# Optimization experiments

Measured on AMD Instinct MI355X. Metric: run time of the kernel, lower is better.

The kernel has to match this reference:

```python
import jax, jax.numpy as jnp
from jax import lax
import numpy as np


def _sym(M):
    return 0.5 * (M + M.T)


def setup_inputs() -> dict:
    key = jax.random.key(0)
    k_a, k_c, k_x = jax.random.split(key, 3)
    dimz, dimx, N = 32, 16, 16384
    A = jax.random.normal(k_a, (dimz, dimz), dtype=jnp.float32)
    A = 0.95 * A / jnp.linalg.norm(A, ord=2)  # stable transition (spectral norm 0.95)
    C = jax.random.normal(k_c, (dimx, dimz), dtype=jnp.float32) / np.float32(np.sqrt(dimz))
    Q = 0.1 * jnp.eye(dimz, dtype=jnp.float32)
    R = 0.1 * jnp.eye(dimx, dtype=jnp.float32)
    m0 = jnp.zeros((dimz, 1), dtype=jnp.float32)
    P0 = jnp.eye(dimz, dtype=jnp.float32)
    x = jax.random.normal(k_x, (dimx, N), dtype=jnp.float32)
    Sigma_AQA = jnp.zeros((dimz, dimz), dtype=jnp.float32)
    Sigma_CRC = jnp.zeros((dimz, dimz), dtype=jnp.float32)
    return {"x": x, "A": A, "C": C, "Q": Q, "R": R, "m0": m0, "P0": P0,
            "Sigma_AQA": Sigma_AQA, "Sigma_CRC": Sigma_CRC}


def _vblds_forward(x, A, C, Q, R, m0, P0, Sigma_AQA, Sigma_CRC):
    dimz = A.shape[0]
    I = jnp.eye(dimz, dtype=x.dtype)

    def woodbury(M, B):
        # I - M (I + B M)^{-1} B   (identity when B == 0, matching module init)
        return I - M @ jnp.linalg.inv(I + B @ M) @ B

    def predict(mu, V):
        G = woodbury(V, Sigma_AQA)
        m = A @ (G @ mu)
        P = A @ G @ V @ A.T + Q
        return m, _sym(P), G

    def update(xn, m, P):
        L = woodbury(P, Sigma_CRC)
        x_hat = C @ (L @ m)
        S_hat = C @ L @ P @ C.T + R
        K = L @ P @ C.T @ jnp.linalg.inv(S_hat)
        mu = L @ m + K @ (xn - x_hat)
        V = (I - K @ C) @ L @ P
        return mu, _sym(V)

    # ---- Kalman filter (sequential recursion via lax.scan) ----
    def filt_step(carry, xn):
        m, P = carry
        mu, V = update(xn, m, P)
        m_next, P_next, _ = predict(mu, V)
        return (m_next, P_next), (mu, V)

    (_, _), (muf, Vf) = lax.scan(filt_step, (m0[:, 0], P0), x.T)  # muf: (N, dz), Vf: (N, dz, dz)

    # ---- RTS smoother (reverse scan) ----
    def smooth_step(carry, inp):
        mu_plus, V_plus = carry
        mufn, Vfn = inp
        m, P, G = predict(mufn, Vfn)
        J = G @ Vfn @ A.T @ jnp.linalg.inv(P)
        mu = G @ mufn + J @ (mu_plus - m)
        V = _sym(G @ Vfn + J @ (V_plus - P) @ J.T)
        V12 = J @ V_plus
        return (mu, V), (mu, V, V12)

    (_, _), (mus_rest, Vs_rest, V12) = lax.scan(
        smooth_step, (muf[-1], Vf[-1]), (muf[:-1], Vf[:-1]), reverse=True)
    mus = jnp.concatenate([mus_rest, muf[-1:]], axis=0)   # (N, dz)
    Vs = jnp.concatenate([Vs_rest, Vf[-1:]], axis=0)      # (N, dz, dz)

    # ---- learn: sufficient statistics and M-step log-likelihood ----
    N = mus.shape[0]
    mu = mus.T  # (dz, N)
    zz = mu @ mu.T + Vs.sum(0)
    z1z1 = mu[:, :-1] @ mu[:, :-1].T + Vs[:-1].sum(0)
    z1z2 = mu[:, :-1] @ mu[:, 1:].T + V12.sum(0)
    z2z2 = mu[:, 1:] @ mu[:, 1:].T + Vs[1:].sum(0)
    zx = mu @ x.T
    xx = x @ x.T

    two_pi = 2.0 * np.float32(np.pi)
    m0_new = mu[:, 0:1]
    P0_new = _sym(Vs[0])
    m0m0 = m0_new @ m0_new.T
    z0m0 = mu[:, 0:1] @ m0_new.T
    z0z0 = mu[:, 0:1] @ mu[:, 0:1].T + Vs[0]
    quad0 = _sym(z0z0 - (z0m0 + z0m0.T) + m0m0)
    ell_z0 = (-0.5 * jnp.linalg.slogdet(two_pi * P0_new)[1]
              - 0.5 * jnp.trace(jnp.linalg.inv(P0_new) @ quad0))

    A_new = z1z2.T @ jnp.linalg.inv(z1z1)
    AzzA = A_new @ z1z1 @ A_new.T
    Az1z2 = A_new @ z1z2
    quadz = _sym(z2z2 - (Az1z2 + Az1z2.T) + AzzA)
    Q_new = quadz / (N - 1)
    ell_z = (-(N - 1) / 2.0 * jnp.linalg.slogdet(two_pi * Q_new)[1]
             - 0.5 * jnp.trace(jnp.linalg.inv(Q_new) @ quadz))

    C_new = zx.T @ jnp.linalg.inv(zz)
    Czx = C_new @ zx
    CzzC = C_new @ zz @ C_new.T
    quadx = _sym(xx - (Czx + Czx.T) + CzzC)
    R_new = quadx / N
    ell_x = (-N / 2.0 * jnp.linalg.slogdet(two_pi * R_new)[1]
             - 0.5 * jnp.trace(jnp.linalg.inv(R_new) @ quadx))

    ell = ell_z + ell_x + ell_z0
    # return in torch layout: (dz, N), (dz, dz, N)
    return (ell, muf.T, jnp.moveaxis(Vf, 0, -1), mus.T,
            jnp.moveaxis(Vs, 0, -1), jnp.moveaxis(V12, 0, -1))


def reference(x, A, C, Q, R, m0, P0, Sigma_AQA, Sigma_CRC):
    return _vblds_forward(x, A, C, Q, R, m0, P0, Sigma_AQA, Sigma_CRC)
```

## Files before the change

kernel.cpp:

```cpp
#include <hip/hip_runtime.h>
#include <math.h>

#define NTT 16384
#define PTOL 1e-5f
#define TCAP 48
#define KTR 32
#define CHL 128
#define NCH 128

static constexpr long O_MUF = 1;
static constexpr long O_VF  = O_MUF + 32L*NTT;
static constexpr long O_MUS = O_VF + 1024L*NTT;
static constexpr long O_VS  = O_MUS + 32L*NTT;
static constexpr long O_V12 = O_VS + 1024L*NTT;

static constexpr long WS_PT  = 0;
static constexpr long WS_PAR = 262144;
static constexpr int PW_VC=0, PW_PC=1024, PW_VSINF=2048, PW_V12INF=3072, PW_INTS=4096;
static constexpr int PW_E=4104, PW_EL=5128, PW_K=6152, PW_SMU=6664;
static constexpr int PW_J=6696, PW_JL=7720, PW_D=8744;
static constexpr int PW_VB=9768, PW_BND=13864, PW_WB=17960, PW_BNDM=22056;
static constexpr int PW_HSVS=26152, PW_HSV12=27176, PW_SVSC=28200, PW_SV12C=29224;
static constexpr long WS_GRAM = WS_PAR + 30248;
static constexpr int  GRAM_STRIDE = 2816;
static constexpr long WS_JT = WS_GRAM;

static constexpr int PB_HEAD = KTR + 1;
static constexpr int PB_FILL = PB_HEAD + TCAP;
static constexpr int PB_MUS  = PB_FILL + 1024;
static constexpr int PB_END  = PB_MUS + NCH;

__device__ __forceinline__ void lbar() {
  asm volatile("s_waitcnt lgkmcnt(0)" ::: "memory");
  __builtin_amdgcn_s_barrier();
}

template<int n>
__device__ __forceinline__ void gj_db(float* a, float* b, int ld, float* ldet) {
  const int tid = threadIdx.x;
  const int nth = blockDim.x;
  for (int k = 0; k < n; ++k) {
    float* src = (k & 1) ? b : a;
    float* dst = (k & 1) ? a : b;
    if (ldet != nullptr && tid == 0) *ldet += logf(fabsf(src[k*ld + k]));
    for (int e = tid; e < 2*n*n; e += nth) {
      int r = e / (2*n), c = e - r*(2*n);
      float piv = src[k*ld + k];
      float pr = src[k*ld + c] / piv;
      float v = (r == k) ? pr : fmaf(-src[r*ld + k], pr, src[r*ld + c]);
      dst[r*ld + c] = v;
    }
    lbar();
  }
}

__device__ __forceinline__ void gj32_256(float* a, float* b) {
  const int tid = threadIdx.x;
  for (int k = 0; k < 32; ++k) {
    float* src = (k & 1) ? b : a;
    float* dst = (k & 1) ? a : b;
    #pragma unroll
    for (int e8 = 0; e8 < 8; ++e8) {
      int e = tid + e8*256;
      int r = e >> 6, c = e & 63;
      float piv = src[k*64 + k];
      float pr = src[k*64 + c] / piv;
      dst[r*64 + c] = (r == k) ? pr : fmaf(-src[r*64 + k], pr, src[r*64 + c]);
    }
    lbar();
  }
}

__device__ __forceinline__ void gj3_db(float* a, float* b, float* ldet0) {
  const int tid = threadIdx.x;
  for (int k = 0; k < 32; ++k) {
    float* src = (k & 1) ? b : a;
    float* dst = (k & 1) ? a : b;
    if (ldet0 != nullptr && tid == 0) *ldet0 += logf(fabsf(src[k*65 + k]));
    #pragma unroll
    for (int e = 0; e < 6; ++e) {
      int ee = tid + e*1024;
      int m = ee >> 11;
      int rr = (ee & 2047) >> 6;
      int c = ee & 63;
      int base = m*2080;
      float piv = src[base + k*65 + k];
      float pr = src[base + k*65 + c] / piv;
      float v = (rr == k) ? pr : fmaf(-src[base + rr*65 + k], pr, src[base + rr*65 + c]);
      dst[base + rr*65 + c] = v;
    }
    lbar();
  }
}

__device__ __forceinline__ void gjzx_db(float* qa, float* qb, float* xa, float* xb,
                                        float* ldz, float* ldx) {
  const int tid = threadIdx.x;
  for (int k = 0; k < 32; ++k) {
    float* qs = (k & 1) ? qb : qa;
    float* qd = (k & 1) ? qa : qb;
    if (tid == 0) *ldz += logf(fabsf(qs[k*65 + k]));
    if (tid == 1 && k < 16) {
      float* xs = (k & 1) ? xb : xa;
      *ldx += logf(fabsf(xs[k*33 + k]));
    }
    #pragma unroll
    for (int e = 0; e < 2; ++e) {
      int ee = tid + e*1024;
      int rr = ee >> 6, c = ee & 63;
      float piv = qs[k*65 + k];
      float pr = qs[k*65 + c] / piv;
      qd[rr*65 + c] = (rr == k) ? pr : fmaf(-qs[rr*65 + k], pr, qs[rr*65 + c]);
    }
    if (k < 16 && tid < 512) {
      float* xs = (k & 1) ? xb : xa;
      float* xd = (k & 1) ? xa : xb;
      int rr = tid >> 5, c = tid & 31;
      float piv = xs[k*33 + k];
      float pr = xs[k*33 + c] / piv;
      xd[rr*33 + c] = (rr == k) ? pr : fmaf(-xs[rr*33 + k], pr, xs[rr*33 + c]);
    }
    lbar();
  }
}

__device__ __forceinline__ double block_sum_d(double p, double* red) {
  #pragma unroll
  for (int o = 32; o > 0; o >>= 1) p += __shfl_down(p, o);
  const int tid = threadIdx.x;
  if ((tid & 63) == 0) red[tid >> 6] = p;
  lbar();
  double s = 0.0;
  if (tid == 0) {
    #pragma unroll
    for (int q = 0; q < 16; ++q) s += red[q];
  }
  lbar();
  return s;
}

__global__ __launch_bounds__(256) void k_ric(
    const float* __restrict__ A, const float* __restrict__ C,
    const float* __restrict__ Q, const float* __restrict__ R,
    const float* __restrict__ m0, const float* __restrict__ P0,
    const float* __restrict__ x, float* __restrict__ out, float* __restrict__ wsp)
{
  __shared__ float sA[1056], sC[528], sQ[1056], sR[272];
  __shared__ float sPa[1056], sPb[1056], sV[1056], sAV[1056];
  __shared__ float sCP[528], sKt[544], sAug[528], sAug2[528];
  __shared__ float sm[32], smu[32], sxh[16], sxt[16];
  __shared__ int s_conv;
  const int tid = threadIdx.x;
  const int j = tid & 31, i8 = tid >> 5;

  for (int e = tid; e < 1024; e += 256) {
    int idx = (e>>5)*33 + (e&31);
    sA[idx] = A[e]; sQ[idx] = Q[e]; sPa[idx] = P0[e];
  }
  for (int e = tid; e < 512; e += 256) sC[(e>>5)*33 + (e&31)] = C[e];
  sR[(tid>>4)*17 + (tid&15)] = R[tid];
  if (tid < 32) sm[tid] = m0[tid];
  float xcur = 0.f, xnxt = 0.f;
  if (tid < 16) { xcur = x[(long)tid*NTT + 0]; xnxt = x[(long)tid*NTT + 1]; }
  __syncthreads();
  float aj[32];
  #pragma unroll
  for (int k = 0; k < 32; ++k) aj[k] = sA[j*33+k];

  float* Pc = sPa; float* Pn = sPb;
  int t = 0;
  for (; t < TCAP; ++t) {
    if (tid < 16) sxt[tid] = xcur;
    {
      float a0 = 0.f, a1 = 0.f;
      #pragma unroll
      for (int k = 0; k < 32; ++k) {
        float pv = Pc[k*33+j];
        a0 = fmaf(sC[i8*33+k], pv, a0);
        a1 = fmaf(sC[(i8+8)*33+k], pv, a1);
      }
      sCP[i8*33+j] = a0; sCP[(i8+8)*33+j] = a1;
    }
    if (tid < 16) {
      float acc = 0.f;
      #pragma unroll
      for (int k = 0; k < 32; ++k) acc = fmaf(sC[tid*33+k], sm[k], acc);
      sxh[tid] = acc;
    }
    lbar();
    {
      int r = tid >> 4, c = tid & 15;
      float acc = sR[r*17+c];
      #pragma unroll
      for (int k = 0; k < 32; ++k) acc = fmaf(sCP[r*33+k], sC[c*33+k], acc);
      sAug[r*33+c] = acc;
      sAug[r*33+16+c] = (r==c) ? 1.f : 0.f;
    }
    lbar();
    for (int k = 0; k < 16; ++k) {
      float* src = (k & 1) ? sAug2 : sAug;
      float* dst = (k & 1) ? sAug : sAug2;
      float piv = src[k*33+k];
      float prc = src[k*33+j] / piv;
      int r0 = i8, r1 = i8 + 8;
      dst[r0*33+j] = (r0==k) ? prc : fmaf(-src[r0*33+k], prc, src[r0*33+j]);
      dst[r1*33+j] = (r1==k) ? prc : fmaf(-src[r1*33+k], prc, src[r1*33+j]);
      lbar();
    }
    {
      float a0 = 0.f, a1 = 0.f;
      #pragma unroll
      for (int k = 0; k < 16; ++k) {
        float cpv = sCP[k*33+j];
        a0 = fmaf(cpv, sAug[k*33+16+i8], a0);
        a1 = fmaf(cpv, sAug[k*33+16+i8+8], a1);
      }
      sKt[j*17+i8] = a0; sKt[j*17+i8+8] = a1;
    }
    lbar();
    if (tid < 32) {
      float acc = sm[tid];
      #pragma unroll
      for (int k = 0; k < 16; ++k) acc = fmaf(sKt[tid*17+k], sxt[k]-sxh[k], acc);
      smu[tid] = acc;
      out[O_MUF + (long)tid*NTT + t] = acc;
    }
    {
      float a0 = Pc[i8*33+j], a1 = Pc[(i8+8)*33+j], a2 = Pc[(i8+16)*33+j], a3 = Pc[(i8+24)*33+j];
      #pragma unroll
      for (int k = 0; k < 16; ++k) {
        float cpv = sCP[k*33+j];
        a0 = fmaf(-sKt[i8*17+k], cpv, a0);
        a1 = fmaf(-sKt[(i8+8)*17+k], cpv, a1);
        a2 = fmaf(-sKt[(i8+16)*17+k], cpv, a2);
        a3 = fmaf(-sKt[(i8+24)*17+k], cpv, a3);
      }
      sV[i8*33+j] = a0; sV[(i8+8)*33+j] = a1; sV[(i8+16)*33+j] = a2; sV[(i8+24)*33+j] = a3;
      out[O_VF + (long)(i8*32+j)*NTT + t] = a0;
      out[O_VF + (long)((i8+8)*32+j)*NTT + t] = a1;
      out[O_VF + (long)((i8+16)*32+j)*NTT + t] = a2;
      out[O_VF + (long)((i8+24)*32+j)*NTT + t] = a3;
    }
    if (tid == 0) s_conv = 1;
    lbar();
    {
      float a0=0.f,a1=0.f,a2=0.f,a3=0.f;
      #pragma unroll
      for (int k = 0; k < 32; ++k) {
        float vv = sV[k*33+j];
        a0 = fmaf(sA[i8*33+k], vv, a0);
        a1 = fmaf(sA[(i8+8)*33+k], vv, a1);
        a2 = fmaf(sA[(i8+16)*33+k], vv, a2);
        a3 = fmaf(sA[(i8+24)*33+k], vv, a3);
      }
      sAV[i8*33+j] = a0; sAV[(i8+8)*33+j] = a1; sAV[(i8+16)*33+j] = a2; sAV[(i8+24)*33+j] = a3;
    }
    if (tid < 16) { xcur = xnxt; xnxt = x[(long)tid*NTT + t + 2]; }
    lbar();
    {
      float a0 = sQ[i8*33+j], a1 = sQ[(i8+8)*33+j], a2 = sQ[(i8+16)*33+j], a3 = sQ[(i8+24)*33+j];
      #pragma unroll
      for (int k = 0; k < 32; ++k) {
        float av = aj[k];
        a0 = fmaf(sAV[i8*33+k], av, a0);
        a1 = fmaf(sAV[(i8+8)*33+k], av, a1);
        a2 = fmaf(sAV[(i8+16)*33+k], av, a2);
        a3 = fmaf(sAV[(i8+24)*33+k], av, a3);
      }
      Pn[i8*33+j] = a0; Pn[(i8+8)*33+j] = a1; Pn[(i8+16)*33+j] = a2; Pn[(i8+24)*33+j] = a3;
      if (fabsf(a0 - Pc[i8*33+j]) > PTOL || fabsf(a1 - Pc[(i8+8)*33+j]) > PTOL ||
          fabsf(a2 - Pc[(i8+16)*33+j]) > PTOL || fabsf(a3 - Pc[(i8+24)*33+j]) > PTOL)
        s_conv = 0;
    }
    if (tid < 32) {
      float acc = 0.f;
      #pragma unroll
      for (int k = 0; k < 32; ++k) acc = fmaf(sA[tid*33+k], smu[k], acc);
      sm[tid] = acc;
    }
    lbar();
    int sc = s_conv;
    float* sw = Pc; Pc = Pn; Pn = sw;
    if (sc) { ++t; break; }
  }

  const int t_star = t;
  if (tid == 0) ((int*)(wsp + PW_INTS))[0] = t_star;
  #pragma unroll
  for (int m = 0; m < 4; ++m) {
    int r = i8 + 8*m;
    wsp[PW_VC + r*32 + j] = sV[r*33+j];
    wsp[PW_PC + r*32 + j] = Pc[r*33+j];
  }
  if (tid < 32) wsp[PW_SMU + tid] = smu[tid];
  { int e = tid;        wsp[PW_K + e] = sKt[(e>>4)*17 + (e&15)];
    e = tid + 256;      wsp[PW_K + e] = sKt[(e>>4)*17 + (e&15)]; }
  {
    float a0=(i8==j)?1.f:0.f, a1=((i8+8)==j)?1.f:0.f, a2=((i8+16)==j)?1.f:0.f, a3=((i8+24)==j)?1.f:0.f;
    #pragma unroll
    for (int k = 0; k < 16; ++k) {
      float cv = sC[k*33+j];
      a0 = fmaf(-sKt[i8*17+k], cv, a0);
      a1 = fmaf(-sKt[(i8+8)*17+k], cv, a1);
      a2 = fmaf(-sKt[(i8+16)*17+k], cv, a2);
      a3 = fmaf(-sKt[(i8+24)*17+k], cv, a3);
    }
    sAV[i8*33+j]=a0; sAV[(i8+8)*33+j]=a1; sAV[(i8+16)*33+j]=a2; sAV[(i8+24)*33+j]=a3;
  }
  lbar();
  {
    float a0=0.f,a1=0.f,a2=0.f,a3=0.f;
    #pragma unroll
    for (int k = 0; k < 32; ++k) {
      float av = sA[k*33+j];
      a0 = fmaf(sAV[i8*33+k], av, a0);
      a1 = fmaf(sAV[(i8+8)*33+k], av, a1);
      a2 = fmaf(sAV[(i8+16)*33+k], av, a2);
      a3 = fmaf(sAV[(i8+24)*33+k], av, a3);
    }
    Pn[i8*33+j]=a0; Pn[(i8+8)*33+j]=a1; Pn[(i8+16)*33+j]=a2; Pn[(i8+24)*33+j]=a3;
  }
  lbar();
  #pragma unroll
  for (int m = 0; m < 4; ++m) { int r = i8+8*m; wsp[PW_E + r*32 + j] = Pn[r*33+j]; }
  {
    float* cur = Pn; float* tmp = sAV;
    for (int it = 0; it < 7; ++it) {
      float a0=0.f,a1=0.f,a2=0.f,a3=0.f;
      #pragma unroll
      for (int k = 0; k < 32; ++k) {
        float vv = cur[k*33+j];
        a0 = fmaf(cur[i8*33+k], vv, a0);
        a1 = fmaf(cur[(i8+8)*33+k], vv, a1);
        a2 = fmaf(cur[(i8+16)*33+k], vv, a2);
        a3 = fmaf(cur[(i8+24)*33+k], vv, a3);
      }
      tmp[i8*33+j]=a0; tmp[(i8+8)*33+j]=a1; tmp[(i8+16)*33+j]=a2; tmp[(i8+24)*33+j]=a3;
      lbar();
      float* sw = cur; cur = tmp; tmp = sw;
    }
    #pragma unroll
    for (int m = 0; m < 4; ++m) { int r = i8+8*m; wsp[PW_EL + r*32 + j] = cur[r*33+j]; }
  }
}

__global__ __launch_bounds__(256) void k_sconst(
    const float* __restrict__ A, float* __restrict__ wsp)
{
  __shared__ float sA[1056], sVc[1056], sPc[1056], sJ[1056], sX[1056], sU[1056], sT[1056];
  __shared__ float augA[2048], augB[2048];
  __shared__ float sMs[8448];
  const int tid = threadIdx.x;
  const int j = tid & 31, i8 = tid >> 5;
  const int t_star = ((const int*)(wsp + PW_INTS))[0];

  for (int e = tid; e < 1024; e += 256) {
    int idx = (e>>5)*33 + (e&31);
    sA[idx] = A[e]; sVc[idx] = wsp[PW_VC + e]; sPc[idx] = wsp[PW_PC + e];
    augA[(e>>5)*64 + (e&31)] = wsp[PW_PC + e];
    augA[(e>>5)*64 + 32 + (e&31)] = ((e>>5) == (e&31)) ? 1.f : 0.f;
  }
  __syncthreads();
  gj32_256(augA, augB);

  {
    float a0=0.f,a1=0.f,a2=0.f,a3=0.f;
    #pragma unroll
    for (int k = 0; k < 32; ++k) {
      float av = sA[j*33+k];
      a0 = fmaf(sVc[i8*33+k], av, a0);
      a1 = fmaf(sVc[(i8+8)*33+k], av, a1);
      a2 = fmaf(sVc[(i8+16)*33+k], av, a2);
      a3 = fmaf(sVc[(i8+24)*33+k], av, a3);
    }
    sT[i8*33+j]=a0; sT[(i8+8)*33+j]=a1; sT[(i8+16)*33+j]=a2; sT[(i8+24)*33+j]=a3;
  }
  lbar();
  {
    float a0=0.f,a1=0.f,a2=0.f,a3=0.f;
    #pragma unroll
    for (int k = 0; k < 32; ++k) {
      float pv = augA[k*64+32+j];
      a0 = fmaf(sT[i8*33+k], pv, a0);
      a1 = fmaf(sT[(i8+8)*33+k], pv, a1);
      a2 = fmaf(sT[(i8+16)*33+k], pv, a2);
      a3 = fmaf(sT[(i8+24)*33+k], pv, a3);
    }
    sJ[i8*33+j]=a0; sJ[(i8+8)*33+j]=a1; sJ[(i8+16)*33+j]=a2; sJ[(i8+24)*33+j]=a3;
  }
  lbar();
  #pragma unroll
  for (int m = 0; m < 4; ++m) { int r = i8+8*m; wsp[PW_J + r*32 + j] = sJ[r*33+j]; sMs[r*33+j] = sJ[r*33+j]; }
  {
    float a0=(i8==j)?1.f:0.f, a1=((i8+8)==j)?1.f:0.f, a2=((i8+16)==j)?1.f:0.f, a3=((i8+24)==j)?1.f:0.f;
    float b0=0.f,b1=0.f,b2=0.f,b3=0.f;
    #pragma unroll
    for (int k = 0; k < 32; ++k) {
      float av = sA[k*33+j];
      float pv = sPc[k*33+j];
      a0 = fmaf(-sJ[i8*33+k], av, a0);      b0 = fmaf(sJ[i8*33+k], pv, b0);
      a1 = fmaf(-sJ[(i8+8)*33+k], av, a1);  b1 = fmaf(sJ[(i8+8)*33+k], pv, b1);
      a2 = fmaf(-sJ[(i8+16)*33+k], av, a2); b2 = fmaf(sJ[(i8+16)*33+k], pv, b2);
      a3 = fmaf(-sJ[(i8+24)*33+k], av, a3); b3 = fmaf(sJ[(i8+24)*33+k], pv, b3);
    }
    wsp[PW_D + i8*32+j]=a0; wsp[PW_D + (i8+8)*32+j]=a1; wsp[PW_D + (i8+16)*32+j]=a2; wsp[PW_D + (i8+24)*32+j]=a3;
    sT[i8*33+j]=b0; sT[(i8+8)*33+j]=b1; sT[(i8+16)*33+j]=b2; sT[(i8+24)*33+j]=b3;
  }
  lbar();
  {
    float a0=sVc[i8*33+j], a1=sVc[(i8+8)*33+j], a2=sVc[(i8+16)*33+j], a3=sVc[(i8+24)*33+j];
    #pragma unroll
    for (int k = 0; k < 32; ++k) {
      float jv = sJ[j*33+k];
      a0 = fmaf(-sT[i8*33+k], jv, a0);
      a1 = fmaf(-sT[(i8+8)*33+k], jv, a1);
      a2 = fmaf(-sT[(i8+16)*33+k], jv, a2);
      a3 = fmaf(-sT[(i8+24)*33+k], jv, a3);
    }
    sX[i8*33+j]=a0; sX[(i8+8)*33+j]=a1; sX[(i8+16)*33+j]=a2; sX[(i8+24)*33+j]=a3;
  }
  lbar();
  for (int l = 0; l < 8; ++l) {
    const float* Ml = sMs + l*1056;
    {
      float a0=0.f,a1=0.f,a2=0.f,a3=0.f;
      #pragma unroll
      for (int k = 0; k < 32; ++k) {
        float xv = sX[k*33+j];
        a0 = fmaf(Ml[i8*33+k], xv, a0);
        a1 = fmaf(Ml[(i8+8)*33+k], xv, a1);
        a2 = fmaf(Ml[(i8+16)*33+k], xv, a2);
        a3 = fmaf(Ml[(i8+24)*33+k], xv, a3);
      }
      sU[i8*33+j]=a0; sU[(i8+8)*33+j]=a1; sU[(i8+16)*33+j]=a2; sU[(i8+24)*33+j]=a3;
    }
    lbar();
    {
      float a0=sX[i8*33+j], a1=sX[(i8+8)*33+j], a2=sX[(i8+16)*33+j], a3=sX[(i8+24)*33+j];
      float b0=0.f,b1=0.f,b2=0.f,b3=0.f;
      #pragma unroll
      for (int k = 0; k < 32; ++k) {
        float jv = Ml[j*33+k];
        float mv = Ml[k*33+j];
        a0 = fmaf(sU[i8*33+k], jv, a0);       b0 = fmaf(Ml[i8*33+k], mv, b0);
        a1 = fmaf(sU[(i8+8)*33+k], jv, a1);   b1 = fmaf(Ml[(i8+8)*33+k], mv, b1);
        a2 = fmaf(sU[(i8+16)*33+k], jv, a2);  b2 = fmaf(Ml[(i8+16)*33+k], mv, b2);
        a3 = fmaf(sU[(i8+24)*33+k], jv, a3);  b3 = fmaf(Ml[(i8+24)*33+k], mv, b3);
      }
      sX[i8*33+j]=a0; sX[(i8+8)*33+j]=a1; sX[(i8+16)*33+j]=a2; sX[(i8+24)*33+j]=a3;
      if (l < 7) {
        float* Mn = sMs + (l+1)*1056;
        Mn[i8*33+j]=b0; Mn[(i8+8)*33+j]=b1; Mn[(i8+16)*33+j]=b2; Mn[(i8+24)*33+j]=b3;
      }
    }
    lbar();
  }
  #pragma unroll
  for (int m = 0; m < 4; ++m) {
    int r = i8+8*m;
    wsp[PW_VSINF + r*32 + j] = sX[r*33+j];
    wsp[PW_JL + r*32 + j] = sMs[7*1056 + r*33+j];
  }
  float* sXd = augB;
  #pragma unroll
  for (int m = 0; m < 4; ++m) { int r = i8+8*m; sXd[r*33+j] = sVc[r*33+j] - sX[r*33+j]; }
  lbar();
  for (int l = 0; l < 8; ++l) {
    const float* Ml = sMs + l*1056;
    {
      float a0=0.f,a1=0.f,a2=0.f,a3=0.f;
      #pragma unroll
      for (int k = 0; k < 32; ++k) {
        float xv = sXd[k*33+j];
        a0 = fmaf(Ml[i8*33+k], xv, a0);
        a1 = fmaf(Ml[(i8+8)*33+k], xv, a1);
        a2 = fmaf(Ml[(i8+16)*33+k], xv, a2);
        a3 = fmaf(Ml[(i8+24)*33+k], xv, a3);
      }
      sU[i8*33+j]=a0; sU[(i8+8)*33+j]=a1; sU[(i8+16)*33+j]=a2; sU[(i8+24)*33+j]=a3;
    }
    lbar();
    {
      float a0=sXd[i8*33+j], a1=sXd[(i8+8)*33+j], a2=sXd[(i8+16)*33+j], a3=sXd[(i8+24)*33+j];
      #pragma unroll
      for (int k = 0; k < 32; ++k) {
        float jv = Ml[j*33+k];
        a0 = fmaf(sU[i8*33+k], jv, a0);
        a1 = fmaf(sU[(i8+8)*33+k], jv, a1);
        a2 = fmaf(sU[(i8+16)*33+k], jv, a2);
        a3 = fmaf(sU[(i8+24)*33+k], jv, a3);
      }
      sXd[i8*33+j]=a0; sXd[(i8+8)*33+j]=a1; sXd[(i8+16)*33+j]=a2; sXd[(i8+24)*33+j]=a3;
    }
    lbar();
  }
  {
    float a0=0.f,a1=0.f,a2=0.f,a3=0.f;
    #pragma unroll
    for (int k = 0; k < 32; ++k) {
      float xv = sX[k*33+j];
      a0 = fmaf(sJ[i8*33+k], xv, a0);
      a1 = fmaf(sJ[(i8+8)*33+k], xv, a1);
      a2 = fmaf(sJ[(i8+16)*33+k], xv, a2);
      a3 = fmaf(sJ[(i8+24)*33+k], xv, a3);
    }
    wsp[PW_V12INF + i8*32+j]=a0; wsp[PW_V12INF + (i8+8)*32+j]=a1;
    wsp[PW_V12INF + (i8+16)*32+j]=a2; wsp[PW_V12INF + (i8+24)*32+j]=a3;
  }
  const float nt0 = (float)(NTT - t_star);
  const float nt1 = (float)(NTT - 1 - t_star);
  #pragma unroll
  for (int m = 0; m < 4; ++m) {
    int r = i8+8*m;
    wsp[PW_SVSC + r*32 + j] = nt0*sX[r*33+j] + sXd[r*33+j];
    sT[r*33+j] = nt1*sX[r*33+j] + sXd[r*33+j];
  }
  lbar();
  {
    float a0=0.f,a1=0.f,a2=0.f,a3=0.f;
    #pragma unroll
    for (int k = 0; k < 32; ++k) {
      float tv = sT[k*33+j];
      a0 = fmaf(sJ[i8*33+k], tv, a0);
      a1 = fmaf(sJ[(i8+8)*33+k], tv, a1);
      a2 = fmaf(sJ[(i8+16)*33+k], tv, a2);
      a3 = fmaf(sJ[(i8+24)*33+k], tv, a3);
    }
    wsp[PW_SV12C + i8*32+j]=a0; wsp[PW_SV12C + (i8+8)*32+j]=a1;
    wsp[PW_SV12C + (i8+16)*32+j]=a2; wsp[PW_SV12C + (i8+24)*32+j]=a3;
  }
}

__device__ __forceinline__ float mvp16(const float* m, float v, int b0) {
  float s0=0.f, s1=0.f, s2=0.f, s3=0.f;
  #pragma unroll
  for (int q = 0; q < 4; ++q) {
    s0 = fmaf(m[q],    __shfl(v, b0+q),    s0);
    s1 = fmaf(m[4+q],  __shfl(v, b0+4+q),  s1);
    s2 = fmaf(m[8+q],  __shfl(v, b0+8+q),  s2);
    s3 = fmaf(m[12+q], __shfl(v, b0+12+q), s3);
  }
  return (s0+s1)+(s2+s3);
}
__device__ __forceinline__ float mvp8(const float* m, float v, int b0) {
  float s0=0.f, s1=0.f;
  #pragma unroll
  for (int q = 0; q < 4; ++q) {
    s0 = fmaf(m[q],   __shfl(v, b0+q),   s0);
    s1 = fmaf(m[4+q], __shfl(v, b0+4+q), s1);
  }
  return s0+s1;
}

__global__ __launch_bounds__(64) void k_muf_b1(const float* __restrict__ x, float* __restrict__ wsp) {
  __shared__ float sx[16*(CHL+1)];
  const int lane = threadIdx.x;
  const int t_star = ((const int*)(wsp + PW_INTS))[0];
  const int sb = t_star + (int)blockIdx.x * CHL;
  if (sb >= NTT) return;
  const int len = (NTT - sb < CHL) ? (NTT - sb) : CHL;
  for (int q = 0; q < 16; ++q)
    for (int idx = lane; idx < len; idx += 64)
      sx[q*(CHL+1)+idx] = x[(long)q*NTT + sb + idx];
  const int r = lane & 31, bm = (lane & 32) >> 1, bx = (lane & 32) >> 2;
  float e[16], kx[8];
  #pragma unroll
  for (int q = 0; q < 16; ++q) e[q] = wsp[PW_E + r*32 + bm + q];
  #pragma unroll
  for (int q = 0; q < 8; ++q) kx[q] = wsp[PW_K + r*16 + bx + q];
  lbar();
  float mf = 0.f;
  for (int s = 0; s < len; ++s) {
    float xq = sx[(lane&15)*(CHL+1) + s];
    float acc = mvp16(e, mf, bm) + mvp8(kx, xq, bx);
    acc += __shfl_xor(acc, 32);
    mf = acc;
  }
  if (lane < 32) wsp[PW_VB + (int)blockIdx.x*32 + lane] = mf;
}

__global__ __launch_bounds__(64) void k_muf_comb(float* __restrict__ wsp) {
  __shared__ float svb[NCH*32];
  const int lane = threadIdx.x;
  for (int idx = lane; idx < NCH*32; idx += 64) svb[idx] = wsp[PW_VB + idx];
  const int t_star = ((const int*)(wsp + PW_INTS))[0];
  const int r = lane & 31, bm = (lane & 32) >> 1;
  float el[16];
  #pragma unroll
  for (int q = 0; q < 16; ++q) el[q] = wsp[PW_EL + r*32 + bm + q];
  float m = wsp[PW_SMU + r];
  lbar();
  for (int b = 0; b < NCH; ++b) {
    int sb = t_star + b*CHL;
    if (sb >= NTT) break;
    if (lane < 32) wsp[PW_BND + b*32 + lane] = m;
    if (sb + CHL >= NTT) break;
    float vb = svb[b*32 + r];
    float s = mvp16(el, m, bm);
    s += __shfl_xor(s, 32);
    m = vb + s;
  }
}

__global__ __launch_bounds__(64) void k_muf_b2(const float* __restrict__ x, float* __restrict__ out, float* __restrict__ wsp) {
  __shared__ float sx[16*(CHL+1)];
  const int lane = threadIdx.x;
  const int t_star = ((const int*)(wsp + PW_INTS))[0];
  const int sb = t_star + (int)blockIdx.x * CHL;
  if (sb >= NTT) return;
  const int len = (NTT - sb < CHL) ? (NTT - sb) : CHL;
  for (int q = 0; q < 16; ++q)
    for (int idx = lane; idx < len; idx += 64)
      sx[q*(CHL+1)+idx] = x[(long)q*NTT + sb + idx];
  const int r = lane & 31, bm = (lane & 32) >> 1, bx = (lane & 32) >> 2;
  float e[16], kx[8];
  #pragma unroll
  for (int q = 0; q < 16; ++q) e[q] = wsp[PW_E + r*32 + bm + q];
  #pragma unroll
  for (int q = 0; q < 8; ++q) kx[q] = wsp[PW_K + r*16 + bx + q];
  lbar();
  float mf = wsp[PW_BND + (int)blockIdx.x*32 + r];
  float* po = out + O_MUF + (long)r*NTT + sb;
  for (int s = 0; s < len; ++s) {
    float xq = sx[(lane&15)*(CHL+1) + s];
    float acc = mvp16(e, mf, bm) + mvp8(kx, xq, bx);
    acc += __shfl_xor(acc, 32);
    mf = acc;
    if (lane < 32) po[s] = mf;
  }
}

__global__ __launch_bounds__(1024) void k_par1(
    const float* __restrict__ A, const float* __restrict__ Q,
    float* __restrict__ out, float* __restrict__ ws, float* __restrict__ wsp)
{
  __shared__ float sh[9440];
  const int tid = threadIdx.x;
  const int i = tid >> 5, j = tid & 31;
  const int ij33 = i*33 + j;
  const int b = blockIdx.x;

  if (b < PB_HEAD) {
    const int k = b;
    float* sJ = sh; float* sM = sh+1056; float* sT = sh+2112; float* sDl = sh+3168; float* sVo = sh+4224;
    sJ[ij33] = wsp[PW_J + tid];
    sDl[ij33] = wsp[PW_VC + tid] - wsp[PW_VSINF + tid];
    const float vsi = wsp[PW_VSINF + tid];
    lbar();
    float vs;
    if (k == 0) {
      vs = vsi + sDl[ij33];
    } else {
      sM[ij33] = sJ[ij33];
      lbar();
      int hb = 31 - __builtin_clz((unsigned)k);
      for (int b2 = hb-1; b2 >= 0; --b2) {
        { float acc = 0.f;
          #pragma unroll
          for (int k2 = 0; k2 < 32; ++k2) acc = fmaf(sM[i*33+k2], sM[k2*33+j], acc);
          lbar(); sM[ij33] = acc; lbar(); }
        if ((k >> b2) & 1) {
          float acc = 0.f;
          #pragma unroll
          for (int k2 = 0; k2 < 32; ++k2) acc = fmaf(sM[i*33+k2], sJ[k2*33+j], acc);
          lbar(); sM[ij33] = acc; lbar();
        }
      }
      { float acc = 0.f;
        #pragma unroll
        for (int k2 = 0; k2 < 32; ++k2) acc = fmaf(sM[i*33+k2], sDl[k2*33+j], acc);
        sT[ij33] = acc; }
      lbar();
      { float acc = vsi;
        #pragma unroll
        for (int k2 = 0; k2 < 32; ++k2) acc = fmaf(sT[i*33+k2], sM[j*33+k2], acc);
        vs = acc; }
    }
    out[O_VS + (long)tid*NTT + (NTT-1-k)] = vs;
    sVo[ij33] = vs;
    lbar();
    if (k <= KTR-1) {
      float acc = 0.f;
      #pragma unroll
      for (int k2 = 0; k2 < 32; ++k2) acc = fmaf(sJ[i*33+k2], sVo[k2*33+j], acc);
      out[O_V12 + (long)tid*(NTT-1) + (NTT-2-k)] = acc;
    }
  } else if (b < PB_FILL) {
    const int t_star = ((const int*)(wsp + PW_INTS))[0];
    const int tt = b - PB_HEAD;
    if (tt >= t_star) return;
    float* sA = sh; float* sQ2 = sh+1056; float* sVf = sh+2112; float* sAV = sh+3168; float* sP = sh+4224;
    float* aug = sh+5280; float* aug2 = sh+7360;
    sA[ij33] = A[tid]; sQ2[ij33] = Q[tid];
    sVf[ij33] = out[O_VF + (long)tid*NTT + tt];
    lbar();
    { float acc = 0.f;
      #pragma unroll
      for (int k2 = 0; k2 < 32; ++k2) acc = fmaf(sA[i*33+k2], sVf[k2*33+j], acc);
      sAV[ij33] = acc;
    }
    lbar();
    { float a1 = sQ2[ij33];
      float a2 = sQ2[j*33+i];
      #pragma unroll
      for (int k2 = 0; k2 < 32; ++k2) {
        a1 = fmaf(sAV[i*33+k2], sA[j*33+k2], a1);
        a2 = fmaf(sAV[j*33+k2], sA[i*33+k2], a2);
      }
      float ps = 0.5f*(a1 + a2);
      sP[ij33] = ps;
      aug[i*65+j] = ps; aug[i*65+32+j] = (i==j) ? 1.f : 0.f;
    }
    lbar();
    gj_db<32>(aug, aug2, 65, nullptr);
    { float acc = 0.f;
      #pragma unroll
      for (int k2 = 0; k2 < 32; ++k2) acc = fmaf(sVf[i*33+k2], sA[j*33+k2], acc);
      sAV[ij33] = acc;
    }
    lbar();
    { float acc = 0.f;
      #pragma unroll
      for (int k2 = 0; k2 < 32; ++k2) acc = fmaf(sAV[i*33+k2], aug[k2*65+32+j], acc);
      ws[WS_JT + (long)tt*1024 + tid] = acc;
    }
    ws[WS_PT + (long)tt*1024 + tid] = sP[ij33];
  } else if (b < PB_MUS) {
    const int ij = b - PB_FILL;
    const int t_star = ((const int*)(wsp + PW_INTS))[0];
    const int tb = NTT - 1 - KTR;
    const float vf = wsp[PW_VC + ij];
    const float vs = wsp[PW_VSINF + ij];
    const float v12 = wsp[PW_V12INF + ij];
    float* pvf = out + O_VF + (long)ij*NTT;
    float* pvs = out + O_VS + (long)ij*NTT;
    float* pv12 = out + O_V12 + (long)ij*(NTT-1);
    for (int t2 = t_star + tid; t2 < tb; t2 += 1024) {
      pvf[t2] = vf; pvs[t2] = vs; pv12[t2] = v12;
    }
    for (int t2 = tb + ((t_star + tid - tb) % 1024 + 1024) % 1024; t2 < NTT; t2 += 1024) pvf[t2] = vf;
  } else {
    const int c = b - PB_MUS;
    const int t_star = ((const int*)(wsp + PW_INTS))[0];
    const int te = (NTT-1) - c*CHL;
    if (te <= t_star) return;
    const int ts = (te - CHL > t_star) ? (te - CHL) : t_star;
    const int len = te - ts;
    float* smf = sh;
    if (tid < len) {
      for (int q = 0; q < 32; ++q) smf[q*129 + tid] = out[O_MUF + (long)q*NTT + ts + tid];
    }
    lbar();
    if (tid >= 64) return;
    const int lane = tid;
    const int r = lane & 31, bm = (lane & 32) >> 1;
    float dd[16], jj[16];
    #pragma unroll
    for (int q = 0; q < 16; ++q) { dd[q] = wsp[PW_D + r*32 + bm + q]; jj[q] = wsp[PW_J + r*32 + bm + q]; }
    float z = 0.f;
    for (int tt = len-1; tt >= 0; --tt) {
      float mv = smf[(lane&31)*129 + tt];
      float acc = mvp16(dd, mv, bm) + mvp16(jj, z, bm);
      acc += __shfl_xor(acc, 32);
      z = acc;
    }
    if (lane < 32) wsp[PW_WB + c*32 + lane] = z;
  }
}

__global__ __launch_bounds__(64) void k_mus_comb(float* __restrict__ out, float* __restrict__ wsp) {
  __shared__ float swb[NCH*32];
  const int lane = threadIdx.x;
  for (int idx = lane; idx < NCH*32; idx += 64) swb[idx] = wsp[PW_WB + idx];
  const int t_star = ((const int*)(wsp + PW_INTS))[0];
  const int r = lane & 31, bm = (lane & 32) >> 1;
  float jl[16];
  #pragma unroll
  for (int q = 0; q < 16; ++q) jl[q] = wsp[PW_JL + r*32 + bm + q];
  float m = out[O_MUF + (long)r*NTT + (NTT-1)];
  if (lane < 32) out[O_MUS + (long)lane*NTT + (NTT-1)] = m;
  lbar();
  for (int b = 0; b < NCH; ++b) {
    int te = (NTT-1) - b*CHL;
    if (te <= t_star) break;
    if (lane < 32) wsp[PW_BNDM + b*32 + lane] = m;
    int ts = (te - CHL > t_star) ? (te - CHL) : t_star;
    if (ts <= t_star) break;
    float wb = swb[b*32 + r];
    float s = mvp16(jl, m, bm);
    s += __shfl_xor(s, 32);
    m = wb + s;
  }
}

__global__ __launch_bounds__(64) void k_mus_b2(float* __restrict__ out, float* __restrict__ wsp) {
  __shared__ float smf[32*(CHL+1)];
  const int lane = threadIdx.x;
  const int t_star = ((const int*)(wsp + PW_INTS))[0];
  const int te = (NTT-1) - (int)blockIdx.x*CHL;
  if (te <= t_star) return;
  const int ts = (te - CHL > t_star) ? (te - CHL) : t_star;
  const int len = te - ts;
  for (int q = 0; q < 32; ++q)
    for (int idx = lane; idx < len; idx += 64)
      smf[q*(CHL+1)+idx] = out[O_MUF + (long)q*NTT + ts + idx];
  const int r = lane & 31, bm = (lane & 32) >> 1;
  float dd[16], jj[16];
  #pragma unroll
  for (int q = 0; q < 16; ++q) { dd[q] = wsp[PW_D + r*32 + bm + q]; jj[q] = wsp[PW_J + r*32 + bm + q]; }
  lbar();
  float m = wsp[PW_BNDM + (int)blockIdx.x*32 + r];
  float* po = out + O_MUS + (long)r*NTT;
  for (int tt = len-1; tt >= 0; --tt) {
    float mv = smf[(lane&31)*(CHL+1) + tt];
    float acc = mvp16(dd, mv, bm) + mvp16(jj, m, bm);
    acc += __shfl_xor(acc, 32);
    m = acc;
    if (lane < 32) po[ts+tt] = m;
  }
}

__global__ __launch_bounds__(1024) void k_head_ser(
    const float* __restrict__ A, float* __restrict__ out,
    float* __restrict__ ws, float* __restrict__ wsp)
{
  __shared__ float sA[32*33], sJa[32*33], sJb[32*33], sT1[32*33], sT2[32*33], sVs[32*33];
  __shared__ float smufT[32], sam[32], smsp[32];
  const int tid = threadIdx.x;
  const int i = tid >> 5, j = tid & 31;
  const int ij33 = i*33 + j;
  const int t_star = ((const int*)(wsp + PW_INTS))[0];
  sA[ij33] = A[tid];
  float hsvs = 0.f, hsv12 = 0.f;
  if (t_star > 0) {
    float vsinf = wsp[PW_VSINF + tid];
    int tt = t_star - 1;
    float jc = ws[WS_JT + (long)tt*1024 + tid];
    float pc = ws[WS_PT + (long)tt*1024 + tid];
    float vfc = out[O_VF + (long)tid*NTT + tt];
    float mufc = (tid < 32) ? out[O_MUF + (long)tid*NTT + tt] : 0.f;
    if (tid < 32) smsp[tid] = out[O_MUS + (long)tid*NTT + t_star];
    sVs[ij33] = vsinf;
    sJa[ij33] = jc;
    sT1[ij33] = vsinf - pc;
    if (tid < 32) smufT[tid] = mufc;
    lbar();
    float* Jc = sJa; float* Jn = sJb;
    for (; tt >= 0; --tt) {
      float jN = 0.f, pN = 0.f, vfN = 0.f, mufN = 0.f;
      if (tt > 0) {
        jN = ws[WS_JT + (long)(tt-1)*1024 + tid];
        pN = ws[WS_PT + (long)(tt-1)*1024 + tid];
        vfN = out[O_VF + (long)tid*NTT + (tt-1)];
        if (tid < 32) mufN = out[O_MUF + (long)tid*NTT + (tt-1)];
      }
      {
        float t2 = 0.f, v12 = 0.f;
        #pragma unroll
        for (int k2 = 0; k2 < 32; ++k2) {
          t2  = fmaf(Jc[i*33+k2], sT1[k2*33+j], t2);
          v12 = fmaf(Jc[i*33+k2], sVs[k2*33+j], v12);
        }
        sT2[ij33] = t2;
        out[O_V12 + (long)tid*(NTT-1) + tt] = v12;
        hsv12 += v12;
      }
      if (tid < 32) {
        float a = 0.f;
        #pragma unroll
        for (int k2 = 0; k2 < 32; ++k2) a = fmaf(sA[tid*33+k2], smufT[k2], a);
        sam[tid] = a;
      }
      lbar();
      {
        float vsn = vfc;
        #pragma unroll
        for (int k2 = 0; k2 < 32; ++k2) vsn = fmaf(sT2[i*33+k2], Jc[j*33+k2], vsn);
        out[O_VS + (long)tid*NTT + tt] = vsn;
        hsvs += vsn;
        sVs[ij33] = vsn;
        sT1[ij33] = vsn - pN;
        Jn[ij33] = jN;
      }
      if (tid < 32) {
        float mv = smufT[tid];
        #pragma unroll
        for (int k2 = 0; k2 < 32; ++k2) mv = fmaf(Jc[tid*33+k2], smsp[k2] - sam[k2], mv);
        out[O_MUS + (long)tid*NTT + tt] = mv;
        smsp[tid] = mv;
        smufT[tid] = mufN;
      }
      vfc = vfN;
      { float* sw = Jc; Jc = Jn; Jn = sw; }
      lbar();
    }
  }
  wsp[PW_HSVS + tid] = hsvs;
  wsp[PW_HSV12 + tid] = hsv12;
}

__global__ __launch_bounds__(256) void k_gram(const float* __restrict__ out, const float* __restrict__ x, float* __restrict__ ws) {
  __shared__ float smu[32][257];
  __shared__ float sx[256][16];
  const int b = blockIdx.x;
  const int t0 = b*256;
  for (int e = threadIdx.x; e < 32*257; e += 256) {
    int i2 = e/257, tt = e - i2*257;
    int t = t0 + tt;
    smu[i2][tt] = (t < NTT) ? out[O_MUS + (long)i2*NTT + t] : 0.f;
  }
  for (int e = threadIdx.x; e < 16*256; e += 256) {
    int j2 = e >> 8, tt = e & 255;
    sx[tt][j2] = x[(long)j2*NTT + t0 + tt];
  }
  __syncthreads();
  float* pb = ws + WS_GRAM + (long)b*GRAM_STRIDE;
  const int lim12 = (t0 + 256 <= NTT-1) ? 256 : (NTT-1-t0);
  for (int k = 0; k < 4; ++k) {
    int ij = threadIdx.x + k*256; int i2 = ij>>5, j2 = ij&31;
    float g = 0.f, g12 = 0.f;
    for (int tt = 0; tt < 256; ++tt) g = fmaf(smu[i2][tt], smu[j2][tt], g);
    for (int tt = 0; tt < lim12; ++tt) g12 = fmaf(smu[i2][tt], smu[j2][tt+1], g12);
    pb[ij] = g; pb[1024+ij] = g12;
  }
  for (int k = 0; k < 2; ++k) {
    int ij = threadIdx.x + k*256; int i2 = ij>>4, j2 = ij&15;
    float g = 0.f;
    for (int tt = 0; tt < 256; ++tt) g = fmaf(smu[i2][tt], sx[tt][j2], g);
    pb[2048+ij] = g;
  }
  {
    int ij = threadIdx.x; int i2 = ij>>4, j2 = ij&15;
    float g = 0.f;
    for (int tt = 0; tt < 256; ++tt) g = fmaf(sx[tt][i2], sx[tt][j2], g);
    pb[2560+ij] = g;
  }
}

__global__ __launch_bounds__(1024) void k_final(float* __restrict__ out, float* __restrict__ ws) {
  __shared__ float s_zz[1056], s_z11[1056], s_z12[1056], s_z22[1056];
  __shared__ float s_An[1056], s_T[1056], s_Qz[1056], s_W[1056];
  __shared__ float s_Gx[544], s_xx[272], s_Cn[528], s_U16[528], s_T16[272], s_Qx[272];
  __shared__ float a3[3*2080], b3[3*2080];
  __shared__ float qxa[528], qxb[528];
  __shared__ float s_mu0[32], s_muN[32];
  __shared__ float s_ld[3];
  __shared__ double s_red[16];
  const int tid = threadIdx.x;
  const int i = tid>>5, j = tid&31;
  const int ij33 = i*33+j;
  double ell_acc = 0.0;
  const double L2PI = 1.8378770664093454836;
  const float* wsp = ws + WS_PAR;

  float gall = 0.f, g12 = 0.f;
  for (int b = 0; b < 64; ++b) {
    gall += ws[WS_GRAM + (long)b*GRAM_STRIDE + tid];
    g12  += ws[WS_GRAM + (long)b*GRAM_STRIDE + 1024 + tid];
  }
  float svs  = wsp[PW_HSVS + tid] + wsp[PW_SVSC + tid];
  float sv12 = wsp[PW_HSV12 + tid] + wsp[PW_SV12C + tid];
  float vs0  = out[O_VS + (long)tid*NTT + 0];
  float vsN  = out[O_VS + (long)tid*NTT + (NTT-1)];
  if (tid < 512) { float g = 0.f; for (int b = 0; b < 64; ++b) g += ws[WS_GRAM + (long)b*GRAM_STRIDE + 2048 + tid]; s_Gx[(tid>>4)*17 + (tid&15)] = g; }
  if (tid < 256) { float g = 0.f; for (int b = 0; b < 64; ++b) g += ws[WS_GRAM + (long)b*GRAM_STRIDE + 2560 + tid]; s_xx[(tid>>4)*17 + (tid&15)] = g; }
  if (tid < 32) { s_mu0[tid] = out[O_MUS + (long)tid*NTT + 0]; s_muN[tid] = out[O_MUS + (long)tid*NTT + (NTT-1)]; }
  if (tid < 3) s_ld[tid] = 0.f;
  lbar();
  s_zz[ij33]  = gall + svs;
  s_z11[ij33] = (gall - s_muN[i]*s_muN[j]) + (svs - vsN);
  s_z22[ij33] = (gall - s_mu0[i]*s_mu0[j]) + (svs - vs0);
  s_z12[ij33] = g12 + sv12;
  s_W[ij33]   = vs0;
  lbar();

  {
    float p0n = 0.5f*(s_W[i*33+j] + s_W[j*33+i]);
    float a_  = s_mu0[i]*s_mu0[j];
    float aT  = s_mu0[j]*s_mu0[i];
    float u0  = ((a_ + s_W[ij33]) - (a_ + aT)) + a_;
    s_T[ij33] = u0;
    a3[i*65+j] = p0n;             a3[i*65+32+j] = (i==j) ? 1.f : 0.f;
    a3[2080 + i*65+j] = s_z11[ij33]; a3[2080 + i*65+32+j] = (i==j) ? 1.f : 0.f;
    a3[4160 + i*65+j] = s_zz[ij33];  a3[4160 + i*65+32+j] = (i==j) ? 1.f : 0.f;
  }
  lbar();
  { float q0 = 0.5f*(s_T[i*33+j] + s_T[j*33+i]); s_Qz[ij33] = q0; }
  lbar();
  gj3_db(a3, b3, &s_ld[0]);
  {
    double p = (double)a3[i*65+32+j] * (double)s_Qz[j*33+i];
    double tr = block_sum_d(p, s_red);
    if (tid == 0) ell_acc += -0.5*(32.0*L2PI + (double)s_ld[0]) - 0.5*tr;
  }

  {
    float acc = 0.f;
    #pragma unroll
    for (int k2 = 0; k2 < 32; ++k2) acc = fmaf(s_z12[k2*33+i], a3[2080 + k2*65+32+j], acc);
    s_An[ij33] = acc;
  }
  if (tid < 512) {
    int i16 = tid>>5, j32 = tid&31;
    float acc = 0.f;
    #pragma unroll
    for (int k2 = 0; k2 < 32; ++k2) acc = fmaf(s_Gx[k2*17+i16], a3[4160 + k2*65+32+j32], acc);
    s_Cn[i16*33+j32] = acc;
  }
  lbar();
  {
    float acc = 0.f;
    #pragma unroll
    for (int k2 = 0; k2 < 32; ++k2) acc = fmaf(s_An[i*33+k2], s_z12[k2*33+j], acc);
    s_T[ij33] = acc;
  }
  {
    float acc = 0.f;
    #pragma unroll
    for (int k2 = 0; k2 < 32; ++k2) acc = fmaf(s_An[i*33+k2], s_z11[k2*33+j], acc);
    s_W[ij33] = acc;
  }
  if (tid < 256) {
    int a2 = tid>>4, b2 = tid&15;
    float acc = 0.f;
    #pragma unroll
    for (int k2 = 0; k2 < 32; ++k2) acc = fmaf(s_Cn[a2*33+k2], s_Gx[k2*17+b2], acc);
    s_T16[a2*17+b2] = acc;
  }
  if (tid >= 512) {
    int tt2 = tid - 512;
    int i16 = tt2>>5, j32 = tt2&31;
    float acc = 0.f;
    #pragma unroll
    for (int k2 = 0; k2 < 32; ++k2) acc = fmaf(s_Cn[i16*33+k2], s_zz[k2*33+j32], acc);
    s_U16[i16*33+j32] = acc;
  }
  lbar();
  {
    float azza = 0.f;
    #pragma unroll
    for (int k2 = 0; k2 < 32; ++k2) azza = fmaf(s_W[i*33+k2], s_An[j*33+k2], azza);
    float u = (s_z22[ij33] - (s_T[i*33+j]+s_T[j*33+i])) + azza;
    s_Qz[ij33] = u;
  }
  if (tid < 256) {
    int a2 = tid>>4, b2 = tid&15;
    float czzc = 0.f;
    #pragma unroll
    for (int k2 = 0; k2 < 32; ++k2) czzc = fmaf(s_U16[a2*33+k2], s_Cn[b2*33+k2], czzc);
    float u = (s_xx[a2*17+b2] - (s_T16[a2*17+b2]+s_T16[b2*17+a2])) + czzc;
    s_Qx[a2*17+b2] = u;
  }
  lbar();
  {
    float qz = 0.5f*(s_Qz[i*33+j]+s_Qz[j*33+i]);
    s_T[ij33] = qz;
    a3[i*65+j] = qz/16383.0f; a3[i*65+32+j] = (i==j) ? 1.f : 0.f;
  }
  if (tid < 256) {
    int a2 = tid>>4, b2 = tid&15;
    float qx = 0.5f*(s_Qx[a2*17+b2]+s_Qx[b2*17+a2]);
    s_T16[a2*17+b2] = qx;
    qxa[a2*33+b2] = qx/16384.0f; qxa[a2*33+16+b2] = (a2==b2) ? 1.f : 0.f;
  }
  lbar();
  gjzx_db(a3, b3, qxa, qxb, &s_ld[1], &s_ld[2]);
  {
    double p = (double)a3[i*65+32+j] * (double)s_T[j*33+i];
    double tr = block_sum_d(p, s_red);
    if (tid == 0) ell_acc += -8191.5*(32.0*L2PI + (double)s_ld[1]) - 0.5*tr;
  }
  {
    double p = (i < 16 && j < 16) ? (double)qxa[i*33+16+j] * (double)s_T16[j*17+i] : 0.0;
    double tr = block_sum_d(p, s_red);
    if (tid == 0) {
      ell_acc += -8192.0*(16.0*L2PI + (double)s_ld[2]) - 0.5*tr;
      out[0] = (float)ell_acc;
    }
  }
}

extern "C" void kernel_launch(void* const* d_in, const int* in_sizes, int n_in,
                              void* d_out, int out_size, void* d_ws, size_t ws_size,
                              hipStream_t stream) {
  (void)in_sizes; (void)n_in; (void)out_size; (void)ws_size;
  const float* x  = (const float*)d_in[0];
  const float* A  = (const float*)d_in[1];
  const float* C  = (const float*)d_in[2];
  const float* Q  = (const float*)d_in[3];
  const float* R  = (const float*)d_in[4];
  const float* m0 = (const float*)d_in[5];
  const float* P0 = (const float*)d_in[6];
  float* out = (float*)d_out;
  float* ws  = (float*)d_ws;
  float* wsp = ws + WS_PAR;

  hipLaunchKernelGGL(k_ric, dim3(1), dim3(256), 0, stream, A, C, Q, R, m0, P0, x, out, wsp);
  hipLaunchKernelGGL(k_muf_b1, dim3(NCH), dim3(64), 0, stream, x, wsp);
  hipLaunchKernelGGL(k_sconst, dim3(1), dim3(256), 0, stream, A, wsp);
  hipLaunchKernelGGL(k_muf_comb, dim3(1), dim3(64), 0, stream, wsp);
  hipLaunchKernelGGL(k_muf_b2, dim3(NCH), dim3(64), 0, stream, x, out, wsp);
  hipLaunchKernelGGL(k_par1, dim3(PB_END), dim3(1024), 0, stream, A, Q, out, ws, wsp);
  hipLaunchKernelGGL(k_mus_comb, dim3(1), dim3(64), 0, stream, out, wsp);
  hipLaunchKernelGGL(k_mus_b2, dim3(NCH), dim3(64), 0, stream, out, wsp);
  hipLaunchKernelGGL(k_head_ser, dim3(1), dim3(1024), 0, stream, A, out, ws, wsp);
  hipLaunchKernelGGL(k_gram, dim3(64), dim3(256), 0, stream, out, x, ws);
  hipLaunchKernelGGL(k_final, dim3(1), dim3(1024), 0, stream, out, ws);
}
```

Baseline: 508.6 us.

## Replace chunked scan combine passes with overlapping warm-up chunks and blocked inversion

The forward and backward mean recursions previously ran a three-pass chunked scan: per-chunk partials, then a serial combine kernel, then a second pass. Each chunk now starts its recursion GRD steps earlier from a zero state and relies on the stable steady-state transition to forget that start, which removes the combine and boundary kernels and several launches. The filter step is restructured so the predict covariance is computed directly from P via precomputed CA and fused products. Gauss-Jordan inversion now eliminates 4x4 pivot blocks, cutting the number of barriers per inversion by four. The warm-up is an approximation whose accuracy depends on how fast the transition contracts, and the blocked elimination does no pivoting.

```diff
diff --git a/kernel.cpp b/kernel.cpp
--- a/kernel.cpp
+++ b/kernel.cpp
@@ -6,6 +6,7 @@
 #define TCAP 48
 #define KTR 32
 #define CHL 128
+#define GRD 192
 #define NCH 128
 
 static constexpr long O_MUF = 1;
@@ -17,9 +18,8 @@
 static constexpr long WS_PT  = 0;
 static constexpr long WS_PAR = 262144;
 static constexpr int PW_VC=0, PW_PC=1024, PW_VSINF=2048, PW_V12INF=3072, PW_INTS=4096;
-static constexpr int PW_E=4104, PW_EL=5128, PW_K=6152, PW_SMU=6664;
-static constexpr int PW_J=6696, PW_JL=7720, PW_D=8744;
-static constexpr int PW_VB=9768, PW_BND=13864, PW_WB=17960, PW_BNDM=22056;
+static constexpr int PW_E=4104, PW_K=6152, PW_SMU=6664;
+static constexpr int PW_J=6696, PW_D=8744;
 static constexpr int PW_HSVS=26152, PW_HSV12=27176, PW_SVSC=28200, PW_SV12C=29224;
 static constexpr long WS_GRAM = WS_PAR + 30248;
 static constexpr int  GRAM_STRIDE = 2816;
@@ -35,39 +35,65 @@
   __builtin_amdgcn_s_barrier();
 }
 
-template<int n>
-__device__ __forceinline__ void gj_db(float* a, float* b, int ld, float* ldet) {
-  const int tid = threadIdx.x;
-  const int nth = blockDim.x;
-  for (int k = 0; k < n; ++k) {
-    float* src = (k & 1) ? b : a;
-    float* dst = (k & 1) ? a : b;
-    if (ldet != nullptr && tid == 0) *ldet += logf(fabsf(src[k*ld + k]));
-    for (int e = tid; e < 2*n*n; e += nth) {
-      int r = e / (2*n), c = e - r*(2*n);
-      float piv = src[k*ld + k];
-      float pr = src[k*ld + c] / piv;
-      float v = (r == k) ? pr : fmaf(-src[r*ld + k], pr, src[r*ld + c]);
-      dst[r*ld + c] = v;
-    }
-    lbar();
-  }
-}
-
-__device__ __forceinline__ void gj32_256(float* a, float* b) {
-  const int tid = threadIdx.x;
-  for (int k = 0; k < 32; ++k) {
-    float* src = (k & 1) ? b : a;
-    float* dst = (k & 1) ? a : b;
-    #pragma unroll
-    for (int e8 = 0; e8 < 8; ++e8) {
-      int e = tid + e8*256;
-      int r = e >> 6, c = e & 63;
-      float piv = src[k*64 + k];
-      float pr = src[k*64 + c] / piv;
-      dst[r*64 + c] = (r == k) ? pr : fmaf(-src[r*64 + k], pr, src[r*64 + c]);
-    }
-    lbar();
+__device__ __forceinline__ float inv4f(const float* s, int ld, int k, float* w) {
+  float m[4][8];
+  #pragma unroll
+  for (int r = 0; r < 4; ++r) {
+    #pragma unroll
+    for (int c = 0; c < 4; ++c) m[r][c] = s[(k+r)*ld + k + c];
+    m[r][4] = (r==0)?1.f:0.f; m[r][5] = (r==1)?1.f:0.f;
+    m[r][6] = (r==2)?1.f:0.f; m[r][7] = (r==3)?1.f:0.f;
+  }
+  float det = 1.f;
+  #pragma unroll
+  for (int p = 0; p < 4; ++p) {
+    float pv = m[p][p];
+    det *= pv;
+    float rc = 1.f / pv;
+    #pragma unroll
+    for (int c = 0; c < 8; ++c) m[p][c] *= rc;
+    #pragma unroll
+    for (int r = 0; r < 4; ++r) {
+      if (r == p) continue;
+      float f = m[r][p];
+      #pragma unroll
+      for (int c = 0; c < 8; ++c) m[r][c] = fmaf(-f, m[p][c], m[r][c]);
+    }
+  }
+  #pragma unroll
+  for (int r = 0; r < 4; ++r) {
+    w[r*4+0]=m[r][4]; w[r*4+1]=m[r][5]; w[r*4+2]=m[r][6]; w[r*4+3]=m[r][7];
+  }
+  return det;
+}
+
+template<int NR, int LD>
+__device__ __forceinline__ void gjb4_full(float* a, float* b, int tid, int nth, float* ldet) {
+  float* s = a; float* d = b;
+  const int WDT = 2*NR;
+  for (int kb = 0; kb < NR; kb += 4) {
+    float w[16];
+    float det = inv4f(s, LD, kb, w);
+    if (ldet != nullptr && tid == 0) *ldet += logf(fabsf(det));
+    for (int e = tid; e < NR*WDT; e += nth) {
+      int r = e / WDT, c = e - r*WDT;
+      float v;
+      if ((unsigned)(r - kb) < 4u) {
+        int rr = r - kb;
+        v = w[rr*4+0]*s[kb*LD+c] + w[rr*4+1]*s[(kb+1)*LD+c]
+          + w[rr*4+2]*s[(kb+2)*LD+c] + w[rr*4+3]*s[(kb+3)*LD+c];
+      } else {
+        float s0=s[r*LD+kb], s1=s[r*LD+kb+1], s2=s[r*LD+kb+2], s3=s[r*LD+kb+3];
+        float l0 = s0*w[0]+s1*w[4]+s2*w[8]+s3*w[12];
+        float l1 = s0*w[1]+s1*w[5]+s2*w[9]+s3*w[13];
+        float l2 = s0*w[2]+s1*w[6]+s2*w[10]+s3*w[14];
+        float l3 = s0*w[3]+s1*w[7]+s2*w[11]+s3*w[15];
+        v = s[r*LD+c] - (l0*s[kb*LD+c] + l1*s[(kb+1)*LD+c] + l2*s[(kb+2)*LD+c] + l3*s[(kb+3)*LD+c]);
+      }
+      d[r*LD+c] = v;
+    }
+    lbar();
+    float* t2 = s; s = d; d = t2;
   }
 }
 
@@ -139,19 +165,22 @@
   return s;
 }
 
-__global__ __launch_bounds__(256) void k_ric(
+__global__ __launch_bounds__(256) void k_fwd2(
     const float* __restrict__ A, const float* __restrict__ C,
     const float* __restrict__ Q, const float* __restrict__ R,
     const float* __restrict__ m0, const float* __restrict__ P0,
     const float* __restrict__ x, float* __restrict__ out, float* __restrict__ wsp)
 {
-  __shared__ float sA[1056], sC[528], sQ[1056], sR[272];
-  __shared__ float sPa[1056], sPb[1056], sV[1056], sAV[1056];
-  __shared__ float sCP[528], sKt[544], sAug[528], sAug2[528];
-  __shared__ float sm[32], smu[32], sxh[16], sxt[16];
+  __shared__ float sA[1056], sC[528], sQ[1056], sR[272], sCA[528];
+  __shared__ float sPa[1056], sPb[1056], sV[1056], sT[1056];
+  __shared__ float sW[528], sU1[1056], sU2[544];
+  __shared__ float sSa[528], sSb[528], sZ[528], sZ2[528], sK[544];
+  __shared__ float sm[32], smu[32], sxh[16], sxt[16], sy[16];
+  __shared__ float augA[2080], augB[2080], sMs[8448], sJ[1056], sX[1056], sU[1056], sT3[1056];
   __shared__ int s_conv;
   const int tid = threadIdx.x;
   const int j = tid & 31, i8 = tid >> 5;
+  const int r0 = i8, r1 = i8+8, r2 = i8+16, r3 = i8+24;
 
   for (int e = tid; e < 1024; e += 256) {
     int idx = (e>>5)*33 + (e&31);
@@ -161,263 +190,252 @@
   sR[(tid>>4)*17 + (tid&15)] = R[tid];
   if (tid < 32) sm[tid] = m0[tid];
   float xcur = 0.f, xnxt = 0.f;
-  if (tid < 16) { xcur = x[(long)tid*NTT + 0]; xnxt = x[(long)tid*NTT + 1]; }
+  if (tid < 16) { xcur = x[(long)tid*NTT]; xnxt = x[(long)tid*NTT + 1]; }
   __syncthreads();
   float aj[32];
   #pragma unroll
   for (int k = 0; k < 32; ++k) aj[k] = sA[j*33+k];
+  {
+    float a0=0.f, a1=0.f;
+    #pragma unroll
+    for (int k = 0; k < 32; ++k) {
+      float av = sA[k*33+j];
+      a0 = fmaf(sC[r0*33+k], av, a0);
+      a1 = fmaf(sC[r1*33+k], av, a1);
+    }
+    sCA[r0*33+j] = a0; sCA[r1*33+j] = a1;
+  }
+  if (tid < 16) {
+    float acc = 0.f;
+    #pragma unroll
+    for (int k = 0; k < 32; ++k) acc = fmaf(sC[tid*33+k], sm[k], acc);
+    sxh[tid] = acc;
+  }
+  lbar();
 
   float* Pc = sPa; float* Pn = sPb;
   int t = 0;
   for (; t < TCAP; ++t) {
     if (tid < 16) sxt[tid] = xcur;
     {
-      float a0 = 0.f, a1 = 0.f;
+      float a0=0.f,a1=0.f,a2=0.f,a3=0.f,w0=0.f,w1=0.f;
       #pragma unroll
       for (int k = 0; k < 32; ++k) {
         float pv = Pc[k*33+j];
-        a0 = fmaf(sC[i8*33+k], pv, a0);
-        a1 = fmaf(sC[(i8+8)*33+k], pv, a1);
-      }
-      sCP[i8*33+j] = a0; sCP[(i8+8)*33+j] = a1;
-    }
-    if (tid < 16) {
-      float acc = 0.f;
-      #pragma unroll
-      for (int k = 0; k < 32; ++k) acc = fmaf(sC[tid*33+k], sm[k], acc);
-      sxh[tid] = acc;
+        a0 = fmaf(sA[r0*33+k], pv, a0);
+        a1 = fmaf(sA[r1*33+k], pv, a1);
+        a2 = fmaf(sA[r2*33+k], pv, a2);
+        a3 = fmaf(sA[r3*33+k], pv, a3);
+        w0 = fmaf(sC[r0*33+k], pv, w0);
+        w1 = fmaf(sC[r1*33+k], pv, w1);
+      }
+      sT[r0*33+j]=a0; sT[r1*33+j]=a1; sT[r2*33+j]=a2; sT[r3*33+j]=a3;
+      sW[r0*33+j]=w0; sW[r1*33+j]=w1;
+    }
+    if (t > 0) {
+      if (tid < 32) {
+        float acc = 0.f;
+        #pragma unroll
+        for (int k = 0; k < 32; ++k) acc = fmaf(sA[tid*33+k], smu[k], acc);
+        sm[tid] = acc;
+      } else if (tid < 48) {
+        int q = tid - 32;
+        float acc = 0.f;
+        #pragma unroll
+        for (int k = 0; k < 32; ++k) acc = fmaf(sCA[q*33+k], smu[k], acc);
+        sxh[q] = acc;
+      }
     }
     lbar();
     {
       int r = tid >> 4, c = tid & 15;
       float acc = sR[r*17+c];
       #pragma unroll
-      for (int k = 0; k < 32; ++k) acc = fmaf(sCP[r*33+k], sC[c*33+k], acc);
-      sAug[r*33+c] = acc;
-      sAug[r*33+16+c] = (r==c) ? 1.f : 0.f;
-    }
-    lbar();
-    for (int k = 0; k < 16; ++k) {
-      float* src = (k & 1) ? sAug2 : sAug;
-      float* dst = (k & 1) ? sAug : sAug2;
-      float piv = src[k*33+k];
-      float prc = src[k*33+j] / piv;
-      int r0 = i8, r1 = i8 + 8;
-      dst[r0*33+j] = (r0==k) ? prc : fmaf(-src[r0*33+k], prc, src[r0*33+j]);
-      dst[r1*33+j] = (r1==k) ? prc : fmaf(-src[r1*33+k], prc, src[r1*33+j]);
-      lbar();
+      for (int k = 0; k < 32; ++k) acc = fmaf(sW[r*33+k], sC[c*33+k], acc);
+      sSa[r*33+c] = acc;
+      sSa[r*33+16+c] = (r==c) ? 1.f : 0.f;
     }
     {
-      float a0 = 0.f, a1 = 0.f;
-      #pragma unroll
-      for (int k = 0; k < 16; ++k) {
-        float cpv = sCP[k*33+j];
-        a0 = fmaf(cpv, sAug[k*33+16+i8], a0);
-        a1 = fmaf(cpv, sAug[k*33+16+i8+8], a1);
-      }
-      sKt[j*17+i8] = a0; sKt[j*17+i8+8] = a1;
-    }
-    lbar();
+      float a0=sQ[r0*33+j], a1=sQ[r1*33+j], a2=sQ[r2*33+j], a3=sQ[r3*33+j];
+      #pragma unroll
+      for (int k = 0; k < 32; ++k) {
+        float av = aj[k];
+        a0 = fmaf(sT[r0*33+k], av, a0);
+        a1 = fmaf(sT[r1*33+k], av, a1);
+        a2 = fmaf(sT[r2*33+k], av, a2);
+        a3 = fmaf(sT[r3*33+k], av, a3);
+      }
+      sU1[r0*33+j]=a0; sU1[r1*33+j]=a1; sU1[r2*33+j]=a2; sU1[r3*33+j]=a3;
+    }
+    {
+      int rp = tid >> 4, ci = tid & 15;
+      float b0=0.f, b1=0.f;
+      #pragma unroll
+      for (int k = 0; k < 32; ++k) {
+        float cv = sC[ci*33+k];
+        b0 = fmaf(sT[rp*33+k], cv, b0);
+        b1 = fmaf(sT[(rp+16)*33+k], cv, b1);
+      }
+      sU2[rp*17+ci] = b0; sU2[(rp+16)*17+ci] = b1;
+    }
+    lbar();
+    gjb4_full<16,33>(sSa, sSb, tid, 256, nullptr);
+    {
+      float z0=0.f,z1=0.f,q0=0.f,q1=0.f;
+      #pragma unroll
+      for (int q = 0; q < 16; ++q) {
+        float wv = sW[q*33+j];
+        float u2v = sU2[j*17+q];
+        float s0 = sSa[r0*33+16+q];
+        float s1 = sSa[r1*33+16+q];
+        z0 = fmaf(s0, wv, z0); z1 = fmaf(s1, wv, z1);
+        q0 = fmaf(s0, u2v, q0); q1 = fmaf(s1, u2v, q1);
+      }
+      sZ[r0*33+j]=z0; sZ[r1*33+j]=z1; sZ2[r0*33+j]=q0; sZ2[r1*33+j]=q1;
+    }
+    if (tid < 16) {
+      float acc = 0.f;
+      #pragma unroll
+      for (int q = 0; q < 16; ++q) acc = fmaf(sSa[tid*33+16+q], sxt[q]-sxh[q], acc);
+      sy[tid] = acc;
+    }
+    if (tid == 0) s_conv = 1;
+    lbar();
+    {
+      float v0=Pc[r0*33+j], v1=Pc[r1*33+j], v2=Pc[r2*33+j], v3=Pc[r3*33+j];
+      float p0=sU1[r0*33+j], p1=sU1[r1*33+j], p2=sU1[r2*33+j], p3=sU1[r3*33+j];
+      #pragma unroll
+      for (int q = 0; q < 16; ++q) {
+        float zv = sZ[q*33+j], z2v = sZ2[q*33+j];
+        v0 = fmaf(-sW[q*33+r0], zv, v0);
+        v1 = fmaf(-sW[q*33+r1], zv, v1);
+        v2 = fmaf(-sW[q*33+r2], zv, v2);
+        v3 = fmaf(-sW[q*33+r3], zv, v3);
+        p0 = fmaf(-sU2[r0*17+q], z2v, p0);
+        p1 = fmaf(-sU2[r1*17+q], z2v, p1);
+        p2 = fmaf(-sU2[r2*17+q], z2v, p2);
+        p3 = fmaf(-sU2[r3*17+q], z2v, p3);
+      }
+      sV[r0*33+j]=v0; sV[r1*33+j]=v1; sV[r2*33+j]=v2; sV[r3*33+j]=v3;
+      out[O_VF + (long)(r0*32+j)*NTT + t] = v0;
+      out[O_VF + (long)(r1*32+j)*NTT + t] = v1;
+      out[O_VF + (long)(r2*32+j)*NTT + t] = v2;
+      out[O_VF + (long)(r3*32+j)*NTT + t] = v3;
+      Pn[r0*33+j]=p0; Pn[r1*33+j]=p1; Pn[r2*33+j]=p2; Pn[r3*33+j]=p3;
+      if (fabsf(p0-Pc[r0*33+j]) > PTOL || fabsf(p1-Pc[r1*33+j]) > PTOL ||
+          fabsf(p2-Pc[r2*33+j]) > PTOL || fabsf(p3-Pc[r3*33+j]) > PTOL) s_conv = 0;
+    }
     if (tid < 32) {
       float acc = sm[tid];
       #pragma unroll
-      for (int k = 0; k < 16; ++k) acc = fmaf(sKt[tid*17+k], sxt[k]-sxh[k], acc);
+      for (int q = 0; q < 16; ++q) acc = fmaf(sW[q*33+tid], sy[q], acc);
       smu[tid] = acc;
       out[O_MUF + (long)tid*NTT + t] = acc;
     }
-    {
-      float a0 = Pc[i8*33+j], a1 = Pc[(i8+8)*33+j], a2 = Pc[(i8+16)*33+j], a3 = Pc[(i8+24)*33+j];
-      #pragma unroll
-      for (int k = 0; k < 16; ++k) {
-        float cpv = sCP[k*33+j];
-        a0 = fmaf(-sKt[i8*17+k], cpv, a0);
-        a1 = fmaf(-sKt[(i8+8)*17+k], cpv, a1);
-        a2 = fmaf(-sKt[(i8+16)*17+k], cpv, a2);
-        a3 = fmaf(-sKt[(i8+24)*17+k], cpv, a3);
-      }
-      sV[i8*33+j] = a0; sV[(i8+8)*33+j] = a1; sV[(i8+16)*33+j] = a2; sV[(i8+24)*33+j] = a3;
-      out[O_VF + (long)(i8*32+j)*NTT + t] = a0;
-      out[O_VF + (long)((i8+8)*32+j)*NTT + t] = a1;
-      out[O_VF + (long)((i8+16)*32+j)*NTT + t] = a2;
-      out[O_VF + (long)((i8+24)*32+j)*NTT + t] = a3;
-    }
-    if (tid == 0) s_conv = 1;
-    lbar();
-    {
-      float a0=0.f,a1=0.f,a2=0.f,a3=0.f;
-      #pragma unroll
-      for (int k = 0; k < 32; ++k) {
-        float vv = sV[k*33+j];
-        a0 = fmaf(sA[i8*33+k], vv, a0);
-        a1 = fmaf(sA[(i8+8)*33+k], vv, a1);
-        a2 = fmaf(sA[(i8+16)*33+k], vv, a2);
-        a3 = fmaf(sA[(i8+24)*33+k], vv, a3);
-      }
-      sAV[i8*33+j] = a0; sAV[(i8+8)*33+j] = a1; sAV[(i8+16)*33+j] = a2; sAV[(i8+24)*33+j] = a3;
-    }
     if (tid < 16) { xcur = xnxt; xnxt = x[(long)tid*NTT + t + 2]; }
     lbar();
-    {
-      float a0 = sQ[i8*33+j], a1 = sQ[(i8+8)*33+j], a2 = sQ[(i8+16)*33+j], a3 = sQ[(i8+24)*33+j];
-      #pragma unroll
-      for (int k = 0; k < 32; ++k) {
-        float av = aj[k];
-        a0 = fmaf(sAV[i8*33+k], av, a0);
-        a1 = fmaf(sAV[(i8+8)*33+k], av, a1);
-        a2 = fmaf(sAV[(i8+16)*33+k], av, a2);
-        a3 = fmaf(sAV[(i8+24)*33+k], av, a3);
-      }
-      Pn[i8*33+j] = a0; Pn[(i8+8)*33+j] = a1; Pn[(i8+16)*33+j] = a2; Pn[(i8+24)*33+j] = a3;
-      if (fabsf(a0 - Pc[i8*33+j]) > PTOL || fabsf(a1 - Pc[(i8+8)*33+j]) > PTOL ||
-          fabsf(a2 - Pc[(i8+16)*33+j]) > PTOL || fabsf(a3 - Pc[(i8+24)*33+j]) > PTOL)
-        s_conv = 0;
-    }
-    if (tid < 32) {
-      float acc = 0.f;
-      #pragma unroll
-      for (int k = 0; k < 32; ++k) acc = fmaf(sA[tid*33+k], smu[k], acc);
-      sm[tid] = acc;
-    }
-    lbar();
     int sc = s_conv;
-    float* sw = Pc; Pc = Pn; Pn = sw;
+    { float* sw = Pc; Pc = Pn; Pn = sw; }
     if (sc) { ++t; break; }
   }
 
   const int t_star = t;
   if (tid == 0) ((int*)(wsp + PW_INTS))[0] = t_star;
-  #pragma unroll
-  for (int m = 0; m < 4; ++m) {
-    int r = i8 + 8*m;
-    wsp[PW_VC + r*32 + j] = sV[r*33+j];
-    wsp[PW_PC + r*32 + j] = Pc[r*33+j];
-  }
+  wsp[PW_VC + r0*32+j] = sV[r0*33+j]; wsp[PW_VC + r1*32+j] = sV[r1*33+j];
+  wsp[PW_VC + r2*32+j] = sV[r2*33+j]; wsp[PW_VC + r3*32+j] = sV[r3*33+j];
+  wsp[PW_PC + r0*32+j] = Pc[r0*33+j]; wsp[PW_PC + r1*32+j] = Pc[r1*33+j];
+  wsp[PW_PC + r2*32+j] = Pc[r2*33+j]; wsp[PW_PC + r3*32+j] = Pc[r3*33+j];
   if (tid < 32) wsp[PW_SMU + tid] = smu[tid];
-  { int e = tid;        wsp[PW_K + e] = sKt[(e>>4)*17 + (e&15)];
-    e = tid + 256;      wsp[PW_K + e] = sKt[(e>>4)*17 + (e&15)]; }
-  {
-    float a0=(i8==j)?1.f:0.f, a1=((i8+8)==j)?1.f:0.f, a2=((i8+16)==j)?1.f:0.f, a3=((i8+24)==j)?1.f:0.f;
-    #pragma unroll
-    for (int k = 0; k < 16; ++k) {
-      float cv = sC[k*33+j];
-      a0 = fmaf(-sKt[i8*17+k], cv, a0);
-      a1 = fmaf(-sKt[(i8+8)*17+k], cv, a1);
-      a2 = fmaf(-sKt[(i8+16)*17+k], cv, a2);
-      a3 = fmaf(-sKt[(i8+24)*17+k], cv, a3);
-    }
-    sAV[i8*33+j]=a0; sAV[(i8+8)*33+j]=a1; sAV[(i8+16)*33+j]=a2; sAV[(i8+24)*33+j]=a3;
-  }
-  lbar();
+  {
+    int rp = tid >> 4, ci = tid & 15;
+    float k0=0.f, k1=0.f;
+    #pragma unroll
+    for (int q = 0; q < 16; ++q) {
+      float sv = sSa[q*33+16+ci];
+      k0 = fmaf(sW[q*33+rp], sv, k0);
+      k1 = fmaf(sW[q*33+rp+16], sv, k1);
+    }
+    sK[rp*17+ci]=k0; sK[(rp+16)*17+ci]=k1;
+    wsp[PW_K + rp*16+ci]=k0; wsp[PW_K + (rp+16)*16+ci]=k1;
+  }
+  lbar();
+  {
+    float e0=sA[r0*33+j], e1=sA[r1*33+j], e2=sA[r2*33+j], e3=sA[r3*33+j];
+    #pragma unroll
+    for (int q = 0; q < 16; ++q) {
+      float cav = sCA[q*33+j];
+      e0 = fmaf(-sK[r0*17+q], cav, e0);
+      e1 = fmaf(-sK[r1*17+q], cav, e1);
+      e2 = fmaf(-sK[r2*17+q], cav, e2);
+      e3 = fmaf(-sK[r3*17+q], cav, e3);
+    }
+    wsp[PW_E + r0*32+j]=e0; wsp[PW_E + r1*32+j]=e1;
+    wsp[PW_E + r2*32+j]=e2; wsp[PW_E + r3*32+j]=e3;
+  }
+  for (int e = tid; e < 2048; e += 256) {
+    int r = e >> 6, c = e & 63;
+    augA[r*65+c] = (c < 32) ? Pc[r*33+c] : ((c-32 == r) ? 1.f : 0.f);
+  }
+  lbar();
+  gjb4_full<32,65>(augA, augB, tid, 256, nullptr);
   {
     float a0=0.f,a1=0.f,a2=0.f,a3=0.f;
+    #pragma unroll
+    for (int k = 0; k < 32; ++k) {
+      float av = aj[k];
+      a0 = fmaf(sV[r0*33+k], av, a0);
+      a1 = fmaf(sV[r1*33+k], av, a1);
+      a2 = fmaf(sV[r2*33+k], av, a2);
+      a3 = fmaf(sV[r3*33+k], av, a3);
+    }
+    sT3[r0*33+j]=a0; sT3[r1*33+j]=a1; sT3[r2*33+j]=a2; sT3[r3*33+j]=a3;
+  }
+  lbar();
+  {
+    float a0=0.f,a1=0.f,a2=0.f,a3=0.f;
+    #pragma unroll
+    for (int k = 0; k < 32; ++k) {
+      float pv = augA[k*65+32+j];
+      a0 = fmaf(sT3[r0*33+k], pv, a0);
+      a1 = fmaf(sT3[r1*33+k], pv, a1);
+      a2 = fmaf(sT3[r2*33+k], pv, a2);
+      a3 = fmaf(sT3[r3*33+k], pv, a3);
+    }
+    sJ[r0*33+j]=a0; sJ[r1*33+j]=a1; sJ[r2*33+j]=a2; sJ[r3*33+j]=a3;
+  }
+  lbar();
+  wsp[PW_J + r0*32+j]=sJ[r0*33+j]; wsp[PW_J + r1*32+j]=sJ[r1*33+j];
+  wsp[PW_J + r2*32+j]=sJ[r2*33+j]; wsp[PW_J + r3*32+j]=sJ[r3*33+j];
+  sMs[r0*33+j]=sJ[r0*33+j]; sMs[r1*33+j]=sJ[r1*33+j];
+  sMs[r2*33+j]=sJ[r2*33+j]; sMs[r3*33+j]=sJ[r3*33+j];
+  {
+    float a0=(r0==j)?1.f:0.f, a1=(r1==j)?1.f:0.f, a2=(r2==j)?1.f:0.f, a3=(r3==j)?1.f:0.f;
+    float b0=0.f,b1=0.f,b2=0.f,b3=0.f;
     #pragma unroll
     for (int k = 0; k < 32; ++k) {
       float av = sA[k*33+j];
-      a0 = fmaf(sAV[i8*33+k], av, a0);
-      a1 = fmaf(sAV[(i8+8)*33+k], av, a1);
-      a2 = fmaf(sAV[(i8+16)*33+k], av, a2);
-      a3 = fmaf(sAV[(i8+24)*33+k], av, a3);
-    }
-    Pn[i8*33+j]=a0; Pn[(i8+8)*33+j]=a1; Pn[(i8+16)*33+j]=a2; Pn[(i8+24)*33+j]=a3;
-  }
-  lbar();
-  #pragma unroll
-  for (int m = 0; m < 4; ++m) { int r = i8+8*m; wsp[PW_E + r*32 + j] = Pn[r*33+j]; }
-  {
-    float* cur = Pn; float* tmp = sAV;
-    for (int it = 0; it < 7; ++it) {
-      float a0=0.f,a1=0.f,a2=0.f,a3=0.f;
-      #pragma unroll
-      for (int k = 0; k < 32; ++k) {
-        float vv = cur[k*33+j];
-        a0 = fmaf(cur[i8*33+k], vv, a0);
-        a1 = fmaf(cur[(i8+8)*33+k], vv, a1);
-        a2 = fmaf(cur[(i8+16)*33+k], vv, a2);
-        a3 = fmaf(cur[(i8+24)*33+k], vv, a3);
-      }
-      tmp[i8*33+j]=a0; tmp[(i8+8)*33+j]=a1; tmp[(i8+16)*33+j]=a2; tmp[(i8+24)*33+j]=a3;
-      lbar();
-      float* sw = cur; cur = tmp; tmp = sw;
-    }
-    #pragma unroll
-    for (int m = 0; m < 4; ++m) { int r = i8+8*m; wsp[PW_EL + r*32 + j] = cur[r*33+j]; }
-  }
-}
-
-__global__ __launch_bounds__(256) void k_sconst(
-    const float* __restrict__ A, float* __restrict__ wsp)
-{
-  __shared__ float sA[1056], sVc[1056], sPc[1056], sJ[1056], sX[1056], sU[1056], sT[1056];
-  __shared__ float augA[2048], augB[2048];
-  __shared__ float sMs[8448];
-  const int tid = threadIdx.x;
-  const int j = tid & 31, i8 = tid >> 5;
-  const int t_star = ((const int*)(wsp + PW_INTS))[0];
-
-  for (int e = tid; e < 1024; e += 256) {
-    int idx = (e>>5)*33 + (e&31);
-    sA[idx] = A[e]; sVc[idx] = wsp[PW_VC + e]; sPc[idx] = wsp[PW_PC + e];
-    augA[(e>>5)*64 + (e&31)] = wsp[PW_PC + e];
-    augA[(e>>5)*64 + 32 + (e&31)] = ((e>>5) == (e&31)) ? 1.f : 0.f;
-  }
-  __syncthreads();
-  gj32_256(augA, augB);
-
-  {
-    float a0=0.f,a1=0.f,a2=0.f,a3=0.f;
-    #pragma unroll
-    for (int k = 0; k < 32; ++k) {
-      float av = sA[j*33+k];
-      a0 = fmaf(sVc[i8*33+k], av, a0);
-      a1 = fmaf(sVc[(i8+8)*33+k], av, a1);
-      a2 = fmaf(sVc[(i8+16)*33+k], av, a2);
-      a3 = fmaf(sVc[(i8+24)*33+k], av, a3);
-    }
-    sT[i8*33+j]=a0; sT[(i8+8)*33+j]=a1; sT[(i8+16)*33+j]=a2; sT[(i8+24)*33+j]=a3;
-  }
-  lbar();
-  {
-    float a0=0.f,a1=0.f,a2=0.f,a3=0.f;
-    #pragma unroll
-    for (int k = 0; k < 32; ++k) {
-      float pv = augA[k*64+32+j];
-      a0 = fmaf(sT[i8*33+k], pv, a0);
-      a1 = fmaf(sT[(i8+8)*33+k], pv, a1);
-      a2 = fmaf(sT[(i8+16)*33+k], pv, a2);
-      a3 = fmaf(sT[(i8+24)*33+k], pv, a3);
-    }
-    sJ[i8*33+j]=a0; sJ[(i8+8)*33+j]=a1; sJ[(i8+16)*33+j]=a2; sJ[(i8+24)*33+j]=a3;
-  }
-  lbar();
-  #pragma unroll
-  for (int m = 0; m < 4; ++m) { int r = i8+8*m; wsp[PW_J + r*32 + j] = sJ[r*33+j]; sMs[r*33+j] = sJ[r*33+j]; }
-  {
-    float a0=(i8==j)?1.f:0.f, a1=((i8+8)==j)?1.f:0.f, a2=((i8+16)==j)?1.f:0.f, a3=((i8+24)==j)?1.f:0.f;
-    float b0=0.f,b1=0.f,b2=0.f,b3=0.f;
-    #pragma unroll
-    for (int k = 0; k < 32; ++k) {
-      float av = sA[k*33+j];
-      float pv = sPc[k*33+j];
-      a0 = fmaf(-sJ[i8*33+k], av, a0);      b0 = fmaf(sJ[i8*33+k], pv, b0);
-      a1 = fmaf(-sJ[(i8+8)*33+k], av, a1);  b1 = fmaf(sJ[(i8+8)*33+k], pv, b1);
-      a2 = fmaf(-sJ[(i8+16)*33+k], av, a2); b2 = fmaf(sJ[(i8+16)*33+k], pv, b2);
-      a3 = fmaf(-sJ[(i8+24)*33+k], av, a3); b3 = fmaf(sJ[(i8+24)*33+k], pv, b3);
-    }
-    wsp[PW_D + i8*32+j]=a0; wsp[PW_D + (i8+8)*32+j]=a1; wsp[PW_D + (i8+16)*32+j]=a2; wsp[PW_D + (i8+24)*32+j]=a3;
-    sT[i8*33+j]=b0; sT[(i8+8)*33+j]=b1; sT[(i8+16)*33+j]=b2; sT[(i8+24)*33+j]=b3;
-  }
-  lbar();
-  {
-    float a0=sVc[i8*33+j], a1=sVc[(i8+8)*33+j], a2=sVc[(i8+16)*33+j], a3=sVc[(i8+24)*33+j];
+      float pv = Pc[k*33+j];
+      a0 = fmaf(-sJ[r0*33+k], av, a0); b0 = fmaf(sJ[r0*33+k], pv, b0);
+      a1 = fmaf(-sJ[r1*33+k], av, a1); b1 = fmaf(sJ[r1*33+k], pv, b1);
+      a2 = fmaf(-sJ[r2*33+k], av, a2); b2 = fmaf(sJ[r2*33+k], pv, b2);
+      a3 = fmaf(-sJ[r3*33+k], av, a3); b3 = fmaf(sJ[r3*33+k], pv, b3);
+    }
+    wsp[PW_D + r0*32+j]=a0; wsp[PW_D + r1*32+j]=a1;
+    wsp[PW_D + r2*32+j]=a2; wsp[PW_D + r3*32+j]=a3;
+    sT3[r0*33+j]=b0; sT3[r1*33+j]=b1; sT3[r2*33+j]=b2; sT3[r3*33+j]=b3;
+  }
+  lbar();
+  {
+    float a0=sV[r0*33+j], a1=sV[r1*33+j], a2=sV[r2*33+j], a3=sV[r3*33+j];
     #pragma unroll
     for (int k = 0; k < 32; ++k) {
       float jv = sJ[j*33+k];
-      a0 = fmaf(-sT[i8*33+k], jv, a0);
-      a1 = fmaf(-sT[(i8+8)*33+k], jv, a1);
-      a2 = fmaf(-sT[(i8+16)*33+k], jv, a2);
-      a3 = fmaf(-sT[(i8+24)*33+k], jv, a3);
-    }
-    sX[i8*33+j]=a0; sX[(i8+8)*33+j]=a1; sX[(i8+16)*33+j]=a2; sX[(i8+24)*33+j]=a3;
+      a0 = fmaf(-sT3[r0*33+k], jv, a0);
+      a1 = fmaf(-sT3[r1*33+k], jv, a1);
+      a2 = fmaf(-sT3[r2*33+k], jv, a2);
+      a3 = fmaf(-sT3[r3*33+k], jv, a3);
+    }
+    sX[r0*33+j]=a0; sX[r1*33+j]=a1; sX[r2*33+j]=a2; sX[r3*33+j]=a3;
   }
   lbar();
   for (int l = 0; l < 8; ++l) {
@@ -427,43 +445,41 @@
       #pragma unroll
       for (int k = 0; k < 32; ++k) {
         float xv = sX[k*33+j];
-        a0 = fmaf(Ml[i8*33+k], xv, a0);
-        a1 = fmaf(Ml[(i8+8)*33+k], xv, a1);
-        a2 = fmaf(Ml[(i8+16)*33+k], xv, a2);
-        a3 = fmaf(Ml[(i8+24)*33+k], xv, a3);
-      }
-      sU[i8*33+j]=a0; sU[(i8+8)*33+j]=a1; sU[(i8+16)*33+j]=a2; sU[(i8+24)*33+j]=a3;
+        a0 = fmaf(Ml[r0*33+k], xv, a0);
+        a1 = fmaf(Ml[r1*33+k], xv, a1);
+        a2 = fmaf(Ml[r2*33+k], xv, a2);
+        a3 = fmaf(Ml[r3*33+k], xv, a3);
+      }
+      sU[r0*33+j]=a0; sU[r1*33+j]=a1; sU[r2*33+j]=a2; sU[r3*33+j]=a3;
     }
     lbar();
     {
-      float a0=sX[i8*33+j], a1=sX[(i8+8)*33+j], a2=sX[(i8+16)*33+j], a3=sX[(i8+24)*33+j];
+      float a0=sX[r0*33+j], a1=sX[r1*33+j], a2=sX[r2*33+j], a3=sX[r3*33+j];
       float b0=0.f,b1=0.f,b2=0.f,b3=0.f;
       #pragma unroll
       for (int k = 0; k < 32; ++k) {
         float jv = Ml[j*33+k];
         float mv = Ml[k*33+j];
-        a0 = fmaf(sU[i8*33+k], jv, a0);       b0 = fmaf(Ml[i8*33+k], mv, b0);
-        a1 = fmaf(sU[(i8+8)*33+k], jv, a1);   b1 = fmaf(Ml[(i8+8)*33+k], mv, b1);
-        a2 = fmaf(sU[(i8+16)*33+k], jv, a2);  b2 = fmaf(Ml[(i8+16)*33+k], mv, b2);
-        a3 = fmaf(sU[(i8+24)*33+k], jv, a3);  b3 = fmaf(Ml[(i8+24)*33+k], mv, b3);
-      }
-      sX[i8*33+j]=a0; sX[(i8+8)*33+j]=a1; sX[(i8+16)*33+j]=a2; sX[(i8+24)*33+j]=a3;
+        a0 = fmaf(sU[r0*33+k], jv, a0); b0 = fmaf(Ml[r0*33+k], mv, b0);
+        a1 = fmaf(sU[r1*33+k], jv, a1); b1 = fmaf(Ml[r1*33+k], mv, b1);
+        a2 = fmaf(sU[r2*33+k], jv, a2); b2 = fmaf(Ml[r2*33+k], mv, b2);
+        a3 = fmaf(sU[r3*33+k], jv, a3); b3 = fmaf(Ml[r3*33+k], mv, b3);
+      }
+      sX[r0*33+j]=a0; sX[r1*33+j]=a1; sX[r2*33+j]=a2; sX[r3*33+j]=a3;
       if (l < 7) {
         float* Mn = sMs + (l+1)*1056;
-        Mn[i8*33+j]=b0; Mn[(i8+8)*33+j]=b1; Mn[(i8+16)*33+j]=b2; Mn[(i8+24)*33+j]=b3;
-      }
-    }
-    lbar();
-  }
-  #pragma unroll
-  for (int m = 0; m < 4; ++m) {
-    int r = i8+8*m;
-    wsp[PW_VSINF + r*32 + j] = sX[r*33+j];
-    wsp[PW_JL + r*32 + j] = sMs[7*1056 + r*33+j];
-  }
+        Mn[r0*33+j]=b0; Mn[r1*33+j]=b1; Mn[r2*33+j]=b2; Mn[r3*33+j]=b3;
+      }
+    }
+    lbar();
+  }
+  wsp[PW_VSINF + r0*32+j]=sX[r0*33+j]; wsp[PW_VSINF + r1*32+j]=sX[r1*33+j];
+  wsp[PW_VSINF + r2*32+j]=sX[r2*33+j]; wsp[PW_VSINF + r3*32+j]=sX[r3*33+j];
   float* sXd = augB;
-  #pragma unroll
-  for (int m = 0; m < 4; ++m) { int r = i8+8*m; sXd[r*33+j] = sVc[r*33+j] - sX[r*33+j]; }
+  sXd[r0*33+j] = sV[r0*33+j] - sX[r0*33+j];
+  sXd[r1*33+j] = sV[r1*33+j] - sX[r1*33+j];
+  sXd[r2*33+j] = sV[r2*33+j] - sX[r2*33+j];
+  sXd[r3*33+j] = sV[r3*33+j] - sX[r3*33+j];
   lbar();
   for (int l = 0; l < 8; ++l) {
     const float* Ml = sMs + l*1056;
@@ -472,25 +488,25 @@
       #pragma unroll
       for (int k = 0; k < 32; ++k) {
         float xv = sXd[k*33+j];
-        a0 = fmaf(Ml[i8*33+k], xv, a0);
-        a1 = fmaf(Ml[(i8+8)*33+k], xv, a1);
-        a2 = fmaf(Ml[(i8+16)*33+k], xv, a2);
-        a3 = fmaf(Ml[(i8+24)*33+k], xv, a3);
-      }
-      sU[i8*33+j]=a0; sU[(i8+8)*33+j]=a1; sU[(i8+16)*33+j]=a2; sU[(i8+24)*33+j]=a3;
+        a0 = fmaf(Ml[r0*33+k], xv, a0);
+        a1 = fmaf(Ml[r1*33+k], xv, a1);
+        a2 = fmaf(Ml[r2*33+k], xv, a2);
+        a3 = fmaf(Ml[r3*33+k], xv, a3);
+      }
+      sU[r0*33+j]=a0; sU[r1*33+j]=a1; sU[r2*33+j]=a2; sU[r3*33+j]=a3;
     }
     lbar();
     {
-      float a0=sXd[i8*33+j], a1=sXd[(i8+8)*33+j], a2=sXd[(i8+16)*33+j], a3=sXd[(i8+24)*33+j];
+      float a0=sXd[r0*33+j], a1=sXd[r1*33+j], a2=sXd[r2*33+j], a3=sXd[r3*33+j];
       #pragma unroll
       for (int k = 0; k < 32; ++k) {
         float jv = Ml[j*33+k];
-        a0 = fmaf(sU[i8*33+k], jv, a0);
-        a1 = fmaf(sU[(i8+8)*33+k], jv, a1);
-        a2 = fmaf(sU[(i8+16)*33+k], jv, a2);
-        a3 = fmaf(sU[(i8+24)*33+k], jv, a3);
-      }
-      sXd[i8*33+j]=a0; sXd[(i8+8)*33+j]=a1; sXd[(i8+16)*33+j]=a2; sXd[(i8+24)*33+j]=a3;
+        a0 = fmaf(sU[r0*33+k], jv, a0);
+        a1 = fmaf(sU[r1*33+k], jv, a1);
+        a2 = fmaf(sU[r2*33+k], jv, a2);
+        a3 = fmaf(sU[r3*33+k], jv, a3);
+      }
+      sXd[r0*33+j]=a0; sXd[r1*33+j]=a1; sXd[r2*33+j]=a2; sXd[r3*33+j]=a3;
     }
     lbar();
   }
@@ -499,35 +515,37 @@
     #pragma unroll
     for (int k = 0; k < 32; ++k) {
       float xv = sX[k*33+j];
-      a0 = fmaf(sJ[i8*33+k], xv, a0);
-      a1 = fmaf(sJ[(i8+8)*33+k], xv, a1);
-      a2 = fmaf(sJ[(i8+16)*33+k], xv, a2);
-      a3 = fmaf(sJ[(i8+24)*33+k], xv, a3);
-    }
-    wsp[PW_V12INF + i8*32+j]=a0; wsp[PW_V12INF + (i8+8)*32+j]=a1;
-    wsp[PW_V12INF + (i8+16)*32+j]=a2; wsp[PW_V12INF + (i8+24)*32+j]=a3;
-  }
-  const float nt0 = (float)(NTT - t_star);
-  const float nt1 = (float)(NTT - 1 - t_star);
-  #pragma unroll
-  for (int m = 0; m < 4; ++m) {
-    int r = i8+8*m;
-    wsp[PW_SVSC + r*32 + j] = nt0*sX[r*33+j] + sXd[r*33+j];
-    sT[r*33+j] = nt1*sX[r*33+j] + sXd[r*33+j];
-  }
+      a0 = fmaf(sJ[r0*33+k], xv, a0);
+      a1 = fmaf(sJ[r1*33+k], xv, a1);
+      a2 = fmaf(sJ[r2*33+k], xv, a2);
+      a3 = fmaf(sJ[r3*33+k], xv, a3);
+    }
+    wsp[PW_V12INF + r0*32+j]=a0; wsp[PW_V12INF + r1*32+j]=a1;
+    wsp[PW_V12INF + r2*32+j]=a2; wsp[PW_V12INF + r3*32+j]=a3;
+  }
+  const float nt0f = (float)(NTT - t_star);
+  const float nt1f = (float)(NTT - 1 - t_star);
+  wsp[PW_SVSC + r0*32+j] = nt0f*sX[r0*33+j] + sXd[r0*33+j];
+  wsp[PW_SVSC + r1*32+j] = nt0f*sX[r1*33+j] + sXd[r1*33+j];
+  wsp[PW_SVSC + r2*32+j] = nt0f*sX[r2*33+j] + sXd[r2*33+j];
+  wsp[PW_SVSC + r3*32+j] = nt0f*sX[r3*33+j] + sXd[r3*33+j];
+  sT3[r0*33+j] = nt1f*sX[r0*33+j] + sXd[r0*33+j];
+  sT3[r1*33+j] = nt1f*sX[r1*33+j] + sXd[r1*33+j];
+  sT3[r2*33+j] = nt1f*sX[r2*33+j] + sXd[r2*33+j];
+  sT3[r3*33+j] = nt1f*sX[r3*33+j] + sXd[r3*33+j];
   lbar();
   {
     float a0=0.f,a1=0.f,a2=0.f,a3=0.f;
     #pragma unroll
     for (int k = 0; k < 32; ++k) {
-      float tv = sT[k*33+j];
-      a0 = fmaf(sJ[i8*33+k], tv, a0);
-      a1 = fmaf(sJ[(i8+8)*33+k], tv, a1);
-      a2 = fmaf(sJ[(i8+16)*33+k], tv, a2);
-      a3 = fmaf(sJ[(i8+24)*33+k], tv, a3);
-    }
-    wsp[PW_SV12C + i8*32+j]=a0; wsp[PW_SV12C + (i8+8)*32+j]=a1;
-    wsp[PW_SV12C + (i8+16)*32+j]=a2; wsp[PW_SV12C + (i8+24)*32+j]=a3;
+      float tv = sT3[k*33+j];
+      a0 = fmaf(sJ[r0*33+k], tv, a0);
+      a1 = fmaf(sJ[r1*33+k], tv, a1);
+      a2 = fmaf(sJ[r2*33+k], tv, a2);
+      a3 = fmaf(sJ[r3*33+k], tv, a3);
+    }
+    wsp[PW_SV12C + r0*32+j]=a0; wsp[PW_SV12C + r1*32+j]=a1;
+    wsp[PW_SV12C + r2*32+j]=a2; wsp[PW_SV12C + r3*32+j]=a3;
   }
 }
 
@@ -552,81 +570,35 @@
   return s0+s1;
 }
 
-__global__ __launch_bounds__(64) void k_muf_b1(const float* __restrict__ x, float* __restrict__ wsp) {
-  __shared__ float sx[16*(CHL+1)];
+__global__ __launch_bounds__(64) void k_muf(const float* __restrict__ x, float* __restrict__ out, float* __restrict__ wsp) {
+  __shared__ float sx[16*321];
   const int lane = threadIdx.x;
   const int t_star = ((const int*)(wsp + PW_INTS))[0];
   const int sb = t_star + (int)blockIdx.x * CHL;
   if (sb >= NTT) return;
   const int len = (NTT - sb < CHL) ? (NTT - sb) : CHL;
+  int gs = (blockIdx.x == 0) ? sb : sb - GRD;
+  if (gs < 0) gs = 0;
+  const int total = sb + len - gs;
   for (int q = 0; q < 16; ++q)
-    for (int idx = lane; idx < len; idx += 64)
-      sx[q*(CHL+1)+idx] = x[(long)q*NTT + sb + idx];
+    for (int idx = lane; idx < total; idx += 64)
+      sx[q*321 + idx] = x[(long)q*NTT + gs + idx];
   const int r = lane & 31, bm = (lane & 32) >> 1, bx = (lane & 32) >> 2;
   float e[16], kx[8];
   #pragma unroll
   for (int q = 0; q < 16; ++q) e[q] = wsp[PW_E + r*32 + bm + q];
   #pragma unroll
   for (int q = 0; q < 8; ++q) kx[q] = wsp[PW_K + r*16 + bx + q];
-  lbar();
-  float mf = 0.f;
-  for (int s = 0; s < len; ++s) {
-    float xq = sx[(lane&15)*(CHL+1) + s];
+  float mf = (blockIdx.x == 0) ? wsp[PW_SMU + r] : 0.f;
+  lbar();
+  float* po = out + O_MUF + (long)r*NTT;
+  for (int s = 0; s < total; ++s) {
+    float xq = sx[(lane&15)*321 + s];
     float acc = mvp16(e, mf, bm) + mvp8(kx, xq, bx);
     acc += __shfl_xor(acc, 32);
     mf = acc;
-  }
-  if (lane < 32) wsp[PW_VB + (int)blockIdx.x*32 + lane] = mf;
-}
-
-__global__ __launch_bounds__(64) void k_muf_comb(float* __restrict__ wsp) {
-  __shared__ float svb[NCH*32];
-  const int lane = threadIdx.x;
-  for (int idx = lane; idx < NCH*32; idx += 64) svb[idx] = wsp[PW_VB + idx];
-  const int t_star = ((const int*)(wsp + PW_INTS))[0];
-  const int r = lane & 31, bm = (lane & 32) >> 1;
-  float el[16];
-  #pragma unroll
-  for (int q = 0; q < 16; ++q) el[q] = wsp[PW_EL + r*32 + bm + q];
-  float m = wsp[PW_SMU + r];
-  lbar();
-  for (int b = 0; b < NCH; ++b) {
-    int sb = t_star + b*CHL;
-    if (sb >= NTT) break;
-    if (lane < 32) wsp[PW_BND + b*32 + lane] = m;
-    if (sb + CHL >= NTT) break;
-    float vb = svb[b*32 + r];
-    float s = mvp16(el, m, bm);
-    s += __shfl_xor(s, 32);
-    m = vb + s;
-  }
-}
-
-__global__ __launch_bounds__(64) void k_muf_b2(const float* __restrict__ x, float* __restrict__ out, float* __restrict__ wsp) {
-  __shared__ float sx[16*(CHL+1)];
-  const int lane = threadIdx.x;
-  const int t_star = ((const int*)(wsp + PW_INTS))[0];
-  const int sb = t_star + (int)blockIdx.x * CHL;
-  if (sb >= NTT) return;
-  const int len = (NTT - sb < CHL) ? (NTT - sb) : CHL;
-  for (int q = 0; q < 16; ++q)
-    for (int idx = lane; idx < len; idx += 64)
-      sx[q*(CHL+1)+idx] = x[(long)q*NTT + sb + idx];
-  const int r = lane & 31, bm = (lane & 32) >> 1, bx = (lane & 32) >> 2;
-  float e[16], kx[8];
-  #pragma unroll
-  for (int q = 0; q < 16; ++q) e[q] = wsp[PW_E + r*32 + bm + q];
-  #pragma unroll
-  for (int q = 0; q < 8; ++q) kx[q] = wsp[PW_K + r*16 + bx + q];
-  lbar();
-  float mf = wsp[PW_BND + (int)blockIdx.x*32 + r];
-  float* po = out + O_MUF + (long)r*NTT + sb;
-  for (int s = 0; s < len; ++s) {
-    float xq = sx[(lane&15)*(CHL+1) + s];
-    float acc = mvp16(e, mf, bm) + mvp8(kx, xq, bx);
-    acc += __shfl_xor(acc, 32);
-    mf = acc;
-    if (lane < 32) po[s] = mf;
+    int tg = gs + s;
+    if (tg >= sb && lane < 32) po[tg] = mf;
   }
 }
 
@@ -634,11 +606,12 @@
     const float* __restrict__ A, const float* __restrict__ Q,
     float* __restrict__ out, float* __restrict__ ws, float* __restrict__ wsp)
 {
-  __shared__ float sh[9440];
+  __shared__ float sh[10400];
   const int tid = threadIdx.x;
   const int i = tid >> 5, j = tid & 31;
   const int ij33 = i*33 + j;
   const int b = blockIdx.x;
+  const int t_star = ((const int*)(wsp + PW_INTS))[0];
 
   if (b < PB_HEAD) {
     const int k = b;
@@ -686,7 +659,6 @@
       out[O_V12 + (long)tid*(NTT-1) + (NTT-2-k)] = acc;
     }
   } else if (b < PB_FILL) {
-    const int t_star = ((const int*)(wsp + PW_INTS))[0];
     const int tt = b - PB_HEAD;
     if (tt >= t_star) return;
     float* sA = sh; float* sQ2 = sh+1056; float* sVf = sh+2112; float* sAV = sh+3168; float* sP = sh+4224;
@@ -712,7 +684,7 @@
       aug[i*65+j] = ps; aug[i*65+32+j] = (i==j) ? 1.f : 0.f;
     }
     lbar();
-    gj_db<32>(aug, aug2, 65, nullptr);
+    gjb4_full<32,65>(aug, aug2, tid, 1024, nullptr);
     { float acc = 0.f;
       #pragma unroll
       for (int k2 = 0; k2 < 32; ++k2) acc = fmaf(sVf[i*33+k2], sA[j*33+k2], acc);
@@ -727,7 +699,6 @@
     ws[WS_PT + (long)tt*1024 + tid] = sP[ij33];
   } else if (b < PB_MUS) {
     const int ij = b - PB_FILL;
-    const int t_star = ((const int*)(wsp + PW_INTS))[0];
     const int tb = NTT - 1 - KTR;
     const float vf = wsp[PW_VC + ij];
     const float vs = wsp[PW_VSINF + ij];
@@ -735,20 +706,20 @@
     float* pvf = out + O_VF + (long)ij*NTT;
     float* pvs = out + O_VS + (long)ij*NTT;
     float* pv12 = out + O_V12 + (long)ij*(NTT-1);
-    for (int t2 = t_star + tid; t2 < tb; t2 += 1024) {
-      pvf[t2] = vf; pvs[t2] = vs; pv12[t2] = v12;
-    }
-    for (int t2 = tb + ((t_star + tid - tb) % 1024 + 1024) % 1024; t2 < NTT; t2 += 1024) pvf[t2] = vf;
+    for (int t2 = t_star + tid; t2 < NTT; t2 += 1024) pvf[t2] = vf;
+    for (int t2 = t_star + tid; t2 < tb; t2 += 1024) { pvs[t2] = vs; pv12[t2] = v12; }
   } else {
     const int c = b - PB_MUS;
-    const int t_star = ((const int*)(wsp + PW_INTS))[0];
     const int te = (NTT-1) - c*CHL;
     if (te <= t_star) return;
     const int ts = (te - CHL > t_star) ? (te - CHL) : t_star;
-    const int len = te - ts;
+    int start = te + GRD;
+    if (start > NTT-1) start = NTT-1;
+    const int total = start - ts + 1;
     float* smf = sh;
-    if (tid < len) {
-      for (int q = 0; q < 32; ++q) smf[q*129 + tid] = out[O_MUF + (long)q*NTT + ts + tid];
+    for (int e = tid; e < 32*total; e += 1024) {
+      int q = e / total, idx = e - q*total;
+      smf[q*321 + idx] = out[O_MUF + (long)q*NTT + ts + idx];
     }
     lbar();
     if (tid >= 64) return;
@@ -757,66 +728,20 @@
     float dd[16], jj[16];
     #pragma unroll
     for (int q = 0; q < 16; ++q) { dd[q] = wsp[PW_D + r*32 + bm + q]; jj[q] = wsp[PW_J + r*32 + bm + q]; }
-    float z = 0.f;
-    for (int tt = len-1; tt >= 0; --tt) {
-      float mv = smf[(lane&31)*129 + tt];
-      float acc = mvp16(dd, mv, bm) + mvp16(jj, z, bm);
+    float m;
+    if (start == NTT-1) {
+      m = smf[r*321 + (total-1)];
+      if (c == 0 && lane < 32) out[O_MUS + (long)r*NTT + (NTT-1)] = m;
+    } else {
+      m = 0.f;
+    }
+    for (int tt = start-1; tt >= ts; --tt) {
+      float mv = smf[r*321 + (tt - ts)];
+      float acc = mvp16(dd, mv, bm) + mvp16(jj, m, bm);
       acc += __shfl_xor(acc, 32);
-      z = acc;
-    }
-    if (lane < 32) wsp[PW_WB + c*32 + lane] = z;
-  }
-}
-
-__global__ __launch_bounds__(64) void k_mus_comb(float* __restrict__ out, float* __restrict__ wsp) {
-  __shared__ float swb[NCH*32];
-  const int lane = threadIdx.x;
-  for (int idx = lane; idx < NCH*32; idx += 64) swb[idx] = wsp[PW_WB + idx];
-  const int t_star = ((const int*)(wsp + PW_INTS))[0];
-  const int r = lane & 31, bm = (lane & 32) >> 1;
-  float jl[16];
-  #pragma unroll
-  for (int q = 0; q < 16; ++q) jl[q] = wsp[PW_JL + r*32 + bm + q];
-  float m = out[O_MUF + (long)r*NTT + (NTT-1)];
-  if (lane < 32) out[O_MUS + (long)lane*NTT + (NTT-1)] = m;
-  lbar();
-  for (int b = 0; b < NCH; ++b) {
-    int te = (NTT-1) - b*CHL;
-    if (te <= t_star) break;
-    if (lane < 32) wsp[PW_BNDM + b*32 + lane] = m;
-    int ts = (te - CHL > t_star) ? (te - CHL) : t_star;
-    if (ts <= t_star) break;
-    float wb = swb[b*32 + r];
-    float s = mvp16(jl, m, bm);
-    s += __shfl_xor(s, 32);
-    m = wb + s;
-  }
-}
-
-__global__ __launch_bounds__(64) void k_mus_b2(float* __restrict__ out, float* __restrict__ wsp) {
-  __shared__ float smf[32*(CHL+1)];
-  const int lane = threadIdx.x;
-  const int t_star = ((const int*)(wsp + PW_INTS))[0];
-  const int te = (NTT-1) - (int)blockIdx.x*CHL;
-  if (te <= t_star) return;
-  const int ts = (te - CHL > t_star) ? (te - CHL) : t_star;
-  const int len = te - ts;
-  for (int q = 0; q < 32; ++q)
-    for (int idx = lane; idx < len; idx += 64)
-      smf[q*(CHL+1)+idx] = out[O_MUF + (long)q*NTT + ts + idx];
-  const int r = lane & 31, bm = (lane & 32) >> 1;
-  float dd[16], jj[16];
-  #pragma unroll
-  for (int q = 0; q < 16; ++q) { dd[q] = wsp[PW_D + r*32 + bm + q]; jj[q] = wsp[PW_J + r*32 + bm + q]; }
-  lbar();
-  float m = wsp[PW_BNDM + (int)blockIdx.x*32 + r];
-  float* po = out + O_MUS + (long)r*NTT;
-  for (int tt = len-1; tt >= 0; --tt) {
-    float mv = smf[(lane&31)*(CHL+1) + tt];
-    float acc = mvp16(dd, mv, bm) + mvp16(jj, m, bm);
-    acc += __shfl_xor(acc, 32);
-    m = acc;
-    if (lane < 32) po[ts+tt] = m;
+      m = acc;
+      if (tt < te && lane < 32) out[O_MUS + (long)r*NTT + tt] = m;
+    }
   }
 }
 
@@ -1095,14 +1020,9 @@
   float* ws  = (float*)d_ws;
   float* wsp = ws + WS_PAR;
 
-  hipLaunchKernelGGL(k_ric, dim3(1), dim3(256), 0, stream, A, C, Q, R, m0, P0, x, out, wsp);
-  hipLaunchKernelGGL(k_muf_b1, dim3(NCH), dim3(64), 0, stream, x, wsp);
-  hipLaunchKernelGGL(k_sconst, dim3(1), dim3(256), 0, stream, A, wsp);
-  hipLaunchKernelGGL(k_muf_comb, dim3(1), dim3(64), 0, stream, wsp);
-  hipLaunchKernelGGL(k_muf_b2, dim3(NCH), dim3(64), 0, stream, x, out, wsp);
+  hipLaunchKernelGGL(k_fwd2, dim3(1), dim3(256), 0, stream, A, C, Q, R, m0, P0, x, out, wsp);
+  hipLaunchKernelGGL(k_muf, dim3(NCH), dim3(64), 0, stream, x, out, wsp);
   hipLaunchKernelGGL(k_par1, dim3(PB_END), dim3(1024), 0, stream, A, Q, out, ws, wsp);
-  hipLaunchKernelGGL(k_mus_comb, dim3(1), dim3(64), 0, stream, out, wsp);
-  hipLaunchKernelGGL(k_mus_b2, dim3(NCH), dim3(64), 0, stream, out, wsp);
   hipLaunchKernelGGL(k_head_ser, dim3(1), dim3(1024), 0, stream, A, out, ws, wsp);
   hipLaunchKernelGGL(k_gram, dim3(64), dim3(256), 0, stream, out, x, ws);
   hipLaunchKernelGGL(k_final, dim3(1), dim3(1024), 0, stream, out, ws);
```

Result: faster. 484.2 us (-4.8%).
